# Performance work log

Measured on AMD Instinct MI355X. Metric: run time of the kernel, lower is better.

The kernel has to match this reference:

```python
import jax, jax.numpy as jnp
import numpy as np

B, S, D, H = 512, 128, 2, 512


def _lstm_cell(x, h, c, Wih, Whh, bih, bhh):
    # PyTorch gate order: i, f, g, o
    z = x @ Wih.T + h @ Whh.T + bih + bhh
    i, f, g, o = jnp.split(z, 4, axis=-1)
    c = jax.nn.sigmoid(f) * c + jax.nn.sigmoid(i) * jnp.tanh(g)
    h = jax.nn.sigmoid(o) * jnp.tanh(c)
    return h, c


def setup_inputs() -> dict:
    key = jax.random.key(0)
    ks = jax.random.split(key, 18)
    sc = 1.0 / np.sqrt(H)
    u = lambda k, shape: jax.random.uniform(k, shape, jnp.float32, -sc, sc)
    return {
        "inp": jax.random.normal(ks[0], (B, S, D), jnp.float32),
        "enc_Wih": u(ks[1], (4 * H, D)),
        "enc_Whh": u(ks[2], (4 * H, H)),
        "enc_bih": u(ks[3], (4 * H,)),
        "enc_bhh": u(ks[4], (4 * H,)),
        "dec_Wih": u(ks[5], (4 * H, D)),
        "dec_Whh": u(ks[6], (4 * H, H)),
        "dec_bih": u(ks[7], (4 * H,)),
        "dec_bhh": u(ks[8], (4 * H,)),
        "W1": u(ks[9], (H, H)),
        "b1": u(ks[10], (H,)),
        "W2": u(ks[11], (H, H)),
        "b2": u(ks[12], (H,)),
        "v_w": u(ks[13], (H,)),
        "v_b": u(ks[14], (1,)),
        "comb_W": u(ks[15], (H, 2 * H)),
        "comb_b": u(ks[16], (H,)),
    }


def reference(inp, enc_Wih, enc_Whh, enc_bih, enc_bhh,
              dec_Wih, dec_Whh, dec_bih, dec_bhh,
              W1, b1, W2, b2, v_w, v_b, comb_W, comb_b):
    Bb, Ss, _ = inp.shape
    xs = jnp.transpose(inp, (1, 0, 2))  # [S,B,D]

    # --- encoder LSTM (1 layer) ---
    def enc_step(carry, x):
        h, c = carry
        h, c = _lstm_cell(x, h, c, enc_Wih, enc_Whh, enc_bih, enc_bhh)
        return (h, c), h

    h0 = jnp.zeros((Bb, H), inp.dtype)
    (h_enc, c_enc), enc_out = jax.lax.scan(enc_step, (h0, h0), xs)  # enc_out: [S,B,H]

    W1e = enc_out @ W1.T + b1            # [S,B,H]
    enc_bt = jnp.transpose(enc_out, (1, 0, 2))  # [B,S,H]

    # --- pointer decoder ---
    def dec_step(carry, _):
        h, c, cur = carry
        h, c = _lstm_cell(cur, h, c, dec_Wih, dec_Whh, dec_bih, dec_bhh)
        q = h @ W2.T + b2                               # [B,H]
        u = jnp.tanh(W1e + q[None]) @ v_w + v_b[0]      # [S,B]
        a = jax.nn.softmax(u.T, axis=1)                 # [B,S]
        chosen = jnp.argmax(a, axis=1)                  # [B]
        cur = jnp.take_along_axis(inp, chosen[:, None, None], axis=1)[:, 0, :]  # [B,D]
        ctx = jnp.einsum('bs,bsh->bh', a, enc_bt)       # [B,H]
        h = jnp.concatenate([ctx, h], axis=1) @ comb_W.T + comb_b
        return (h, c, cur), a

    cur0 = jnp.full((Bb, D), -1.0, inp.dtype)
    _, outs = jax.lax.scan(dec_step, (h_enc, c_enc, cur0), None, length=Ss)
    return jnp.transpose(outs, (1, 0, 2))  # [B,S,S]
```

## Files before the change

### kernel.cpp

```cpp
#include <hip/hip_runtime.h>

#define PB 512
#define PS 128
#define PD 2
#define PH 512
#define P4H 2048

typedef unsigned int u32;
typedef unsigned short u16;
typedef __attribute__((ext_vector_type(8))) short short8;
typedef __attribute__((ext_vector_type(4))) float f32x4;

__device__ __forceinline__ float fast_sigmoid(float x) {
    return __fdividef(1.0f, 1.0f + __expf(-x));
}
__device__ __forceinline__ float fast_tanh(float x) {
    float ax = fabsf(x);
    float e = __expf(-2.0f * ax);
    float r = __fdividef(1.0f - e, 1.0f + e);
    return x < 0.0f ? -r : r;
}

__device__ __forceinline__ float bf_dec_u(u16 v) { return __uint_as_float((u32)v << 16); }
__device__ __forceinline__ u16 bf_trunc(float v) { return (u16)(__float_as_uint(v) >> 16); }
__device__ __forceinline__ u16 bf_rne(float v) {
    u32 u = __float_as_uint(v);
    return (u16)((u + 0x7FFFu + ((u >> 16) & 1u)) >> 16);
}
__device__ __forceinline__ void bf_split(float v, u16& hi, u16& lo) {
    hi = bf_trunc(v);
    lo = bf_rne(v - bf_dec_u(hi));
}

struct CF32 {
    using T = float;
    static __device__ __forceinline__ float dec(T v) { return v; }
    static __device__ __forceinline__ T enc(float v) { return v; }
    static __device__ __forceinline__ void dec4(const T* p, float* o) {
        float4 v = *(const float4*)p; o[0]=v.x; o[1]=v.y; o[2]=v.z; o[3]=v.w;
    }
};
struct CBF16 {
    using T = u16;
    static __device__ __forceinline__ float dec(T v) { return __uint_as_float((u32)v << 16); }
    static __device__ __forceinline__ T enc(float v) { return bf_rne(v); }
    static __device__ __forceinline__ void dec4(const T* p, float* o) {
        uint2 v = *(const uint2*)p;
        o[0] = __uint_as_float(v.x << 16);
        o[1] = __uint_as_float(v.x & 0xFFFF0000u);
        o[2] = __uint_as_float(v.y << 16);
        o[3] = __uint_as_float(v.y & 0xFFFF0000u);
    }
};

__global__ __launch_bounds__(256) void prep_whh(
    const float* __restrict__ Whh, u16* __restrict__ hi, u16* __restrict__ lo,
    float* __restrict__ f32out)
{
    int np = blockIdx.x;
    int j = np >> 2, g = np & 3;
    const float* src = Whh + (size_t)(g * PH + j) * PH;
    for (int k = threadIdx.x; k < PH; k += 256) {
        float v = src[k];
        u16 h_, l_;
        bf_split(v, h_, l_);
        hi[(size_t)np * PH + k] = h_;
        lo[(size_t)np * PH + k] = l_;
        if (f32out) f32out[(size_t)np * PH + k] = v;
    }
}
__global__ __launch_bounds__(256) void prep_split(
    const float* __restrict__ W, u16* __restrict__ hi, u16* __restrict__ lo, int K)
{
    int n = blockIdx.x;
    const float* src = W + (size_t)n * K;
    for (int k = threadIdx.x; k < K; k += 256) {
        u16 h_, l_;
        bf_split(src[k], h_, l_);
        hi[(size_t)n * K + k] = h_;
        lo[(size_t)n * K + k] = l_;
    }
}
__global__ __launch_bounds__(256) void prep_transpose_split(
    const float* __restrict__ W, u16* __restrict__ hi, u16* __restrict__ lo)
{
    __shared__ float tile[32][33];
    int m0 = blockIdx.x * 32;
    int k0 = blockIdx.y * 32;
    int tx = threadIdx.x & 31, ty = threadIdx.x >> 5;
    #pragma unroll
    for (int i = 0; i < 4; ++i) {
        int k = k0 + ty + i * 8;
        tile[ty + i * 8][tx] = W[(size_t)k * (2 * PH) + m0 + tx];
    }
    __syncthreads();
    #pragma unroll
    for (int i = 0; i < 4; ++i) {
        int m = m0 + ty + i * 8;
        float v = tile[tx][ty + i * 8];
        u16 h_, l_; bf_split(v, h_, l_);
        hi[(size_t)m * PH + k0 + tx] = h_;
        lo[(size_t)m * PH + k0 + tx] = l_;
    }
}
__global__ __launch_bounds__(256) void prep_small(
    const float* __restrict__ Wih, const float* __restrict__ bih,
    const float* __restrict__ bhh, float* __restrict__ wihp, float* __restrict__ bs)
{
    int np = blockIdx.x * 256 + threadIdx.x;
    if (np >= P4H) return;
    int j = np >> 2, g = np & 3;
    int n = g * PH + j;
    wihp[np * 2]     = Wih[(size_t)n * PD];
    wihp[np * 2 + 1] = Wih[(size_t)n * PD + 1];
    bs[np] = bih[n] + bhh[n];
}
__global__ __launch_bounds__(256) void prep_bfused(
    const float* __restrict__ whh_f32p, const float* __restrict__ comb_b,
    const float* __restrict__ bsum_d, float* __restrict__ bf)
{
    int np = blockIdx.x * 4 + (threadIdx.x >> 6);
    int lane = threadIdx.x & 63;
    const float* wr = whh_f32p + (size_t)np * PH + lane * 8;
    const float* cb = comb_b + lane * 8;
    float s = 0.0f;
    #pragma unroll
    for (int i = 0; i < 8; ++i) s += wr[i] * cb[i];
    #pragma unroll
    for (int off = 32; off; off >>= 1) s += __shfl_xor(s, off);
    if (lane == 0) bf[np] = s + bsum_d[np];
}

template<int EXTRA_MODE, int KK>
__global__ __launch_bounds__(256, 2) void lstm_fused32(
    const u16* __restrict__ Whh_hi, const u16* __restrict__ Whh_lo,
    const float* __restrict__ wih_perm, const float* __restrict__ bsum,
    const float* __restrict__ x, int x_stride,
    const float* __restrict__ h_in,
    float* __restrict__ cT,
    float* __restrict__ h_out,
    void* __restrict__ extra, int ex_stride)
{
    __shared__ u16 As_hi[32][72];
    __shared__ u16 As_lo[32][72];
    __shared__ u16 Bs_hi[64][72];
    __shared__ u16 Bs_lo[64][72];

    const int tid = threadIdx.x;
    const int bnp = blockIdx.x * 32;
    const int bb  = blockIdx.y * 64;
    const int w = tid >> 6;
    const int wm = w >> 1, wn = w & 1;
    const int lane = tid & 63;
    const int l15 = lane & 15, lq = lane >> 4;

    f32x4 acc0 = (f32x4)0.0f, acc1 = (f32x4)0.0f;

    for (int k0 = 0; k0 < KK; k0 += 64) {
        {
            int row = tid >> 3, kc = (tid & 7) * 8;
            *(uint4*)&As_hi[row][kc] = *(const uint4*)&Whh_hi[(size_t)(bnp + row) * KK + k0 + kc];
            *(uint4*)&As_lo[row][kc] = *(const uint4*)&Whh_lo[(size_t)(bnp + row) * KK + k0 + kc];
        }
        #pragma unroll
        for (int rep = 0; rep < 4; ++rep) {
            int chunk = tid + rep * 256;
            int row = chunk >> 4, kc = (chunk & 15) * 4;
            float4 v = *(const float4*)&h_in[(size_t)(bb + row) * KK + k0 + kc];
            u16 h0_, l0_, h1_, l1_, h2_, l2_, h3_, l3_;
            bf_split(v.x, h0_, l0_); bf_split(v.y, h1_, l1_);
            bf_split(v.z, h2_, l2_); bf_split(v.w, h3_, l3_);
            *(uint2*)&Bs_hi[row][kc] = make_uint2((u32)h0_ | ((u32)h1_ << 16),
                                                  (u32)h2_ | ((u32)h3_ << 16));
            *(uint2*)&Bs_lo[row][kc] = make_uint2((u32)l0_ | ((u32)l1_ << 16),
                                                  (u32)l2_ | ((u32)l3_ << 16));
        }
        __syncthreads();
        #pragma unroll
        for (int ks = 0; ks < 2; ++ks) {
            int kk = ks * 32 + lq * 8;
            short8 ah, al, bh0, bl0, bh1, bl1;
            {
                int r = wm * 16 + l15;
                ah = *(const short8*)&As_hi[r][kk];
                al = *(const short8*)&As_lo[r][kk];
            }
            {
                int r = wn * 32 + l15;
                bh0 = *(const short8*)&Bs_hi[r][kk];
                bl0 = *(const short8*)&Bs_lo[r][kk];
                bh1 = *(const short8*)&Bs_hi[r + 16][kk];
                bl1 = *(const short8*)&Bs_lo[r + 16][kk];
            }
            acc0 = __builtin_amdgcn_mfma_f32_16x16x32_bf16(ah, bh0, acc0, 0, 0, 0);
            acc0 = __builtin_amdgcn_mfma_f32_16x16x32_bf16(ah, bl0, acc0, 0, 0, 0);
            acc0 = __builtin_amdgcn_mfma_f32_16x16x32_bf16(al, bh0, acc0, 0, 0, 0);
            acc1 = __builtin_amdgcn_mfma_f32_16x16x32_bf16(ah, bh1, acc1, 0, 0, 0);
            acc1 = __builtin_amdgcn_mfma_f32_16x16x32_bf16(ah, bl1, acc1, 0, 0, 0);
            acc1 = __builtin_amdgcn_mfma_f32_16x16x32_bf16(al, bh1, acc1, 0, 0, 0);
        }
        __syncthreads();
    }

    float* Hs = (float*)&As_hi[0][0];
    const int np_loc = wm * 16 + lq * 4;
    const int np = bnp + np_loc;
    const float4 b4 = *(const float4*)&bsum[np];
    const float4 wA = *(const float4*)&wih_perm[np * 2];
    const float4 wB = *(const float4*)&wih_perm[np * 2 + 4];
    const int jg = np >> 2;
    #pragma unroll
    for (int nf = 0; nf < 2; ++nf) {
        int b_loc = wn * 32 + nf * 16 + l15;
        int b = bb + b_loc;
        float x0 = x[b * x_stride];
        float x1 = x[b * x_stride + 1];
        f32x4 a = nf ? acc1 : acc0;
        float zi = a[0] + b4.x + x0 * wA.x + x1 * wA.y;
        float zf = a[1] + b4.y + x0 * wA.z + x1 * wA.w;
        float zg = a[2] + b4.z + x0 * wB.x + x1 * wB.y;
        float zo = a[3] + b4.w + x0 * wB.z + x1 * wB.w;
        float cold = cT[(size_t)jg * PB + b];
        float cv = fast_sigmoid(zf) * cold + fast_sigmoid(zi) * fast_tanh(zg);
        float hv = fast_sigmoid(zo) * fast_tanh(cv);
        cT[(size_t)jg * PB + b] = cv;
        Hs[(np_loc >> 2) * 66 + b_loc] = hv;
    }
    __syncthreads();
    {
        int b_loc = tid & 63, jp = (tid >> 6) * 2;
        int b = bb + b_loc;
        int jbase = bnp >> 2;
        float h0v = Hs[jp * 66 + b_loc];
        float h1v = Hs[(jp + 1) * 66 + b_loc];
        *(float2*)&h_out[(size_t)b * PH + jbase + jp] = make_float2(h0v, h1v);
        if (EXTRA_MODE == 1) {
            u16* e = (u16*)extra;
            *(u32*)&e[(size_t)b * ex_stride + jbase + jp] =
                (u32)bf_rne(h0v) | ((u32)bf_rne(h1v) << 16);
        } else if (EXTRA_MODE == 2) {
            float* e = (float*)extra;
            *(float2*)&e[(size_t)b * ex_stride + jbase + jp] = make_float2(h0v, h1v);
        }
    }
}

__global__ __launch_bounds__(256, 2) void gemm32_f32(
    const u16* __restrict__ Whi, const u16* __restrict__ Wlo,
    const float* __restrict__ act, const float* __restrict__ bias,
    float* __restrict__ out, int K, int ldo)
{
    __shared__ u16 As_hi[32][72];
    __shared__ u16 As_lo[32][72];
    __shared__ u16 Bs_hi[32][72];
    __shared__ u16 Bs_lo[32][72];

    const int tid = threadIdx.x;
    const int bn = blockIdx.x * 32;
    const int bm = blockIdx.y * 32;
    const int w = tid >> 6;
    const int wm = w >> 1, wn = w & 1;
    const int lane = tid & 63, l15 = lane & 15, lq = lane >> 4;

    f32x4 acc = (f32x4)0.0f;

    for (int k0 = 0; k0 < K; k0 += 64) {
        {
            int row = tid >> 3, kc = (tid & 7) * 8;
            *(uint4*)&As_hi[row][kc] = *(const uint4*)&Whi[(size_t)(bn + row) * K + k0 + kc];
            *(uint4*)&As_lo[row][kc] = *(const uint4*)&Wlo[(size_t)(bn + row) * K + k0 + kc];
        }
        #pragma unroll
        for (int rep = 0; rep < 2; ++rep) {
            int chunk = tid + rep * 256;
            int row = chunk >> 4, kc = (chunk & 15) * 4;
            float4 v = *(const float4*)&act[(size_t)(bm + row) * K + k0 + kc];
            u16 h0_, l0_, h1_, l1_, h2_, l2_, h3_, l3_;
            bf_split(v.x, h0_, l0_); bf_split(v.y, h1_, l1_);
            bf_split(v.z, h2_, l2_); bf_split(v.w, h3_, l3_);
            *(uint2*)&Bs_hi[row][kc] = make_uint2((u32)h0_ | ((u32)h1_ << 16),
                                                  (u32)h2_ | ((u32)h3_ << 16));
            *(uint2*)&Bs_lo[row][kc] = make_uint2((u32)l0_ | ((u32)l1_ << 16),
                                                  (u32)l2_ | ((u32)l3_ << 16));
        }
        __syncthreads();
        #pragma unroll
        for (int ks = 0; ks < 2; ++ks) {
            int kk = ks * 32 + lq * 8;
            short8 ah = *(const short8*)&As_hi[wm * 16 + l15][kk];
            short8 al = *(const short8*)&As_lo[wm * 16 + l15][kk];
            short8 bh = *(const short8*)&Bs_hi[wn * 16 + l15][kk];
            short8 bl = *(const short8*)&Bs_lo[wn * 16 + l15][kk];
            acc = __builtin_amdgcn_mfma_f32_16x16x32_bf16(ah, bh, acc, 0, 0, 0);
            acc = __builtin_amdgcn_mfma_f32_16x16x32_bf16(ah, bl, acc, 0, 0, 0);
            acc = __builtin_amdgcn_mfma_f32_16x16x32_bf16(al, bh, acc, 0, 0, 0);
        }
        __syncthreads();
    }

    int m = bm + wn * 16 + l15;
    int n = bn + wm * 16 + lq * 4;
    float4 b4 = bias ? *(const float4*)&bias[n] : make_float4(0.f, 0.f, 0.f, 0.f);
    *(float4*)&out[(size_t)m * ldo + n] =
        make_float4(acc[0] + b4.x, acc[1] + b4.y, acc[2] + b4.z, acc[3] + b4.w);
}

template<int EXTRA_MODE, int KK>
__global__ __launch_bounds__(256) void lstm_fused(
    const u16* __restrict__ Whh_hi, const u16* __restrict__ Whh_lo,
    const float* __restrict__ wih_perm, const float* __restrict__ bsum,
    const float* __restrict__ x, int x_stride,
    const float* __restrict__ h_in,
    float* __restrict__ cT,
    float* __restrict__ h_out,
    void* __restrict__ extra, int ex_stride)
{
    __shared__ u16 As_hi[64][72];
    __shared__ u16 As_lo[64][72];
    __shared__ u16 Bs_hi[64][72];
    __shared__ u16 Bs_lo[64][72];

    const int tid = threadIdx.x;
    const int bb = blockIdx.x * 64;
    const int bn = blockIdx.y * 64;
    const int w = tid >> 6;
    const int wm = w >> 1, wn = w & 1;
    const int lane = tid & 63;
    const int l15 = lane & 15, lq = lane >> 4;

    f32x4 acc[2][2];
    #pragma unroll
    for (int i = 0; i < 2; ++i)
        #pragma unroll
        for (int j = 0; j < 2; ++j)
            acc[i][j] = (f32x4)0.0f;

    for (int k0 = 0; k0 < KK; k0 += 64) {
        #pragma unroll
        for (int rep = 0; rep < 2; ++rep) {
            int chunk = tid + rep * 256;
            int row = chunk >> 3, kc = (chunk & 7) * 8;
            *(uint4*)&As_hi[row][kc] = *(const uint4*)&Whh_hi[(size_t)(bn + row) * KK + k0 + kc];
            *(uint4*)&As_lo[row][kc] = *(const uint4*)&Whh_lo[(size_t)(bn + row) * KK + k0 + kc];
        }
        #pragma unroll
        for (int rep = 0; rep < 4; ++rep) {
            int chunk = tid + rep * 256;
            int row = chunk >> 4, kc = (chunk & 15) * 4;
            float4 v = *(const float4*)&h_in[(size_t)(bb + row) * KK + k0 + kc];
            u16 h0_, l0_, h1_, l1_, h2_, l2_, h3_, l3_;
            bf_split(v.x, h0_, l0_); bf_split(v.y, h1_, l1_);
            bf_split(v.z, h2_, l2_); bf_split(v.w, h3_, l3_);
            *(uint2*)&Bs_hi[row][kc] = make_uint2((u32)h0_ | ((u32)h1_ << 16),
                                                  (u32)h2_ | ((u32)h3_ << 16));
            *(uint2*)&Bs_lo[row][kc] = make_uint2((u32)l0_ | ((u32)l1_ << 16),
                                                  (u32)l2_ | ((u32)l3_ << 16));
        }
        __syncthreads();
        #pragma unroll
        for (int ks = 0; ks < 2; ++ks) {
            int kk = ks * 32 + lq * 8;
            short8 ah[2], al[2], bh[2], bl[2];
            #pragma unroll
            for (int mf = 0; mf < 2; ++mf) {
                int r = wm * 32 + mf * 16 + l15;
                ah[mf] = *(const short8*)&As_hi[r][kk];
                al[mf] = *(const short8*)&As_lo[r][kk];
            }
            #pragma unroll
            for (int nf = 0; nf < 2; ++nf) {
                int r = wn * 32 + nf * 16 + l15;
                bh[nf] = *(const short8*)&Bs_hi[r][kk];
                bl[nf] = *(const short8*)&Bs_lo[r][kk];
            }
            #pragma unroll
            for (int mf = 0; mf < 2; ++mf)
                #pragma unroll
                for (int nf = 0; nf < 2; ++nf) {
                    acc[mf][nf] = __builtin_amdgcn_mfma_f32_16x16x32_bf16(ah[mf], bh[nf], acc[mf][nf], 0, 0, 0);
                    acc[mf][nf] = __builtin_amdgcn_mfma_f32_16x16x32_bf16(ah[mf], bl[nf], acc[mf][nf], 0, 0, 0);
                    acc[mf][nf] = __builtin_amdgcn_mfma_f32_16x16x32_bf16(al[mf], bh[nf], acc[mf][nf], 0, 0, 0);
                }
        }
        __syncthreads();
    }

    float* Hs = (float*)&As_hi[0][0];
    #pragma unroll
    for (int nf = 0; nf < 2; ++nf) {
        int b_loc = wn * 32 + nf * 16 + l15;
        int b = bb + b_loc;
        float x0 = x[b * x_stride];
        float x1 = x[b * x_stride + 1];
        #pragma unroll
        for (int mf = 0; mf < 2; ++mf) {
            int np_loc = wm * 32 + mf * 16 + lq * 4;
            int np = bn + np_loc;
            float4 b4 = *(const float4*)&bsum[np];
            float4 wA = *(const float4*)&wih_perm[np * 2];
            float4 wB = *(const float4*)&wih_perm[np * 2 + 4];
            float zi = acc[mf][nf][0] + b4.x + x0 * wA.x + x1 * wA.y;
            float zf = acc[mf][nf][1] + b4.y + x0 * wA.z + x1 * wA.w;
            float zg = acc[mf][nf][2] + b4.z + x0 * wB.x + x1 * wB.y;
            float zo = acc[mf][nf][3] + b4.w + x0 * wB.z + x1 * wB.w;
            int jg = np >> 2;
            float cold = cT[(size_t)jg * PB + b];
            float cv = fast_sigmoid(zf) * cold + fast_sigmoid(zi) * fast_tanh(zg);
            float hv = fast_sigmoid(zo) * fast_tanh(cv);
            cT[(size_t)jg * PB + b] = cv;
            Hs[(np_loc >> 2) * 66 + b_loc] = hv;
        }
    }
    __syncthreads();
    {
        int b_loc = tid >> 2, jp = (tid & 3) * 4;
        int b = bb + b_loc;
        int jbase = bn >> 2;
        float4 hv4;
        hv4.x = Hs[(jp + 0) * 66 + b_loc];
        hv4.y = Hs[(jp + 1) * 66 + b_loc];
        hv4.z = Hs[(jp + 2) * 66 + b_loc];
        hv4.w = Hs[(jp + 3) * 66 + b_loc];
        *(float4*)&h_out[(size_t)b * PH + jbase + jp] = hv4;
        if (EXTRA_MODE == 1) {
            u16* e = (u16*)extra;
            *(uint2*)&e[(size_t)b * ex_stride + jbase + jp] =
                make_uint2((u32)bf_rne(hv4.x) | ((u32)bf_rne(hv4.y) << 16),
                           (u32)bf_rne(hv4.z) | ((u32)bf_rne(hv4.w) << 16));
        } else if (EXTRA_MODE == 2) {
            float* e = (float*)extra;
            *(float4*)&e[(size_t)b * ex_stride + jbase + jp] = hv4;
        }
    }
}

template<int ACT_F32, int OUTMODE>
__global__ __launch_bounds__(256) void gemm_wtA(
    const u16* __restrict__ Whi, const u16* __restrict__ Wlo,
    const void* __restrict__ act, const float* __restrict__ bias,
    void* __restrict__ out, void* __restrict__ out2, int K, int ldo)
{
    __shared__ u16 As_hi[64][72];
    __shared__ u16 As_lo[64][72];
    __shared__ u16 Bs_hi[64][72];
    __shared__ u16 Bs_lo[64][72];

    const int tid = threadIdx.x;
    const int bm = blockIdx.x * 64;
    const int bn = blockIdx.y * 64;
    const int w = tid >> 6;
    const int wm = w >> 1, wn = w & 1;
    const int lane = tid & 63;
    const int l15 = lane & 15, lq = lane >> 4;

    f32x4 acc[2][2];
    #pragma unroll
    for (int i = 0; i < 2; ++i)
        #pragma unroll
        for (int j = 0; j < 2; ++j)
            acc[i][j] = (f32x4)0.0f;

    for (int k0 = 0; k0 < K; k0 += 64) {
        #pragma unroll
        for (int rep = 0; rep < 2; ++rep) {
            int chunk = tid + rep * 256;
            int row = chunk >> 3, kc = (chunk & 7) * 8;
            *(uint4*)&As_hi[row][kc] = *(const uint4*)&Whi[(size_t)(bn + row) * K + k0 + kc];
            *(uint4*)&As_lo[row][kc] = *(const uint4*)&Wlo[(size_t)(bn + row) * K + k0 + kc];
        }
        if (ACT_F32) {
            const float* a = (const float*)act;
            #pragma unroll
            for (int rep = 0; rep < 4; ++rep) {
                int chunk = tid + rep * 256;
                int row = chunk >> 4, kc = (chunk & 15) * 4;
                float4 v = *(const float4*)&a[(size_t)(bm + row) * K + k0 + kc];
                u16 h0_, l0_, h1_, l1_, h2_, l2_, h3_, l3_;
                bf_split(v.x, h0_, l0_); bf_split(v.y, h1_, l1_);
                bf_split(v.z, h2_, l2_); bf_split(v.w, h3_, l3_);
                *(uint2*)&Bs_hi[row][kc] = make_uint2((u32)h0_ | ((u32)h1_ << 16),
                                                      (u32)h2_ | ((u32)h3_ << 16));
                *(uint2*)&Bs_lo[row][kc] = make_uint2((u32)l0_ | ((u32)l1_ << 16),
                                                      (u32)l2_ | ((u32)l3_ << 16));
            }
        } else {
            const u16* a = (const u16*)act;
            #pragma unroll
            for (int rep = 0; rep < 2; ++rep) {
                int chunk = tid + rep * 256;
                int row = chunk >> 3, kc = (chunk & 7) * 8;
                *(uint4*)&Bs_hi[row][kc] = *(const uint4*)&a[(size_t)(bm + row) * K + k0 + kc];
            }
        }
        __syncthreads();
        #pragma unroll
        for (int ks = 0; ks < 2; ++ks) {
            int kk = ks * 32 + lq * 8;
            short8 ah[2], al[2], bh[2], bl[2];
            #pragma unroll
            for (int mf = 0; mf < 2; ++mf) {
                int r = wm * 32 + mf * 16 + l15;
                ah[mf] = *(const short8*)&As_hi[r][kk];
                al[mf] = *(const short8*)&As_lo[r][kk];
            }
            #pragma unroll
            for (int nf = 0; nf < 2; ++nf) {
                int r = wn * 32 + nf * 16 + l15;
                bh[nf] = *(const short8*)&Bs_hi[r][kk];
                if (ACT_F32) bl[nf] = *(const short8*)&Bs_lo[r][kk];
            }
            #pragma unroll
            for (int mf = 0; mf < 2; ++mf)
                #pragma unroll
                for (int nf = 0; nf < 2; ++nf) {
                    acc[mf][nf] = __builtin_amdgcn_mfma_f32_16x16x32_bf16(ah[mf], bh[nf], acc[mf][nf], 0, 0, 0);
                    if (ACT_F32) {
                        acc[mf][nf] = __builtin_amdgcn_mfma_f32_16x16x32_bf16(ah[mf], bl[nf], acc[mf][nf], 0, 0, 0);
                        acc[mf][nf] = __builtin_amdgcn_mfma_f32_16x16x32_bf16(al[mf], bh[nf], acc[mf][nf], 0, 0, 0);
                    } else {
                        acc[mf][nf] = __builtin_amdgcn_mfma_f32_16x16x32_bf16(al[mf], bh[nf], acc[mf][nf], 0, 0, 0);
                    }
                }
        }
        __syncthreads();
    }

    #pragma unroll
    for (int nf = 0; nf < 2; ++nf) {
        int m = bm + wn * 32 + nf * 16 + l15;
        #pragma unroll
        for (int mf = 0; mf < 2; ++mf) {
            int n = bn + wm * 32 + mf * 16 + lq * 4;
            float4 b4 = bias ? *(const float4*)&bias[n] : make_float4(0.f, 0.f, 0.f, 0.f);
            float v0 = acc[mf][nf][0] + b4.x;
            float v1 = acc[mf][nf][1] + b4.y;
            float v2 = acc[mf][nf][2] + b4.z;
            float v3 = acc[mf][nf][3] + b4.w;
            if (OUTMODE == 1) {
                u16* o = (u16*)out;
                *(uint2*)&o[(size_t)m * ldo + n] =
                    make_uint2((u32)bf_rne(v0) | ((u32)bf_rne(v1) << 16),
                               (u32)bf_rne(v2) | ((u32)bf_rne(v3) << 16));
            } else if (OUTMODE == 2) {
                u16 h0_, l0_, h1_, l1_, h2_, l2_, h3_, l3_;
                bf_split(v0, h0_, l0_); bf_split(v1, h1_, l1_);
                bf_split(v2, h2_, l2_); bf_split(v3, h3_, l3_);
                u16* oh = (u16*)out;
                u16* ol = (u16*)out2;
                *(uint2*)&oh[(size_t)m * ldo + n] =
                    make_uint2((u32)h0_ | ((u32)h1_ << 16), (u32)h2_ | ((u32)h3_ << 16));
                *(uint2*)&ol[(size_t)m * ldo + n] =
                    make_uint2((u32)l0_ | ((u32)l1_ << 16), (u32)l2_ | ((u32)l3_ << 16));
            } else {
                float* o = (float*)out;
                *(float4*)&o[(size_t)m * ldo + n] = make_float4(v0, v1, v2, v3);
            }
        }
    }
}

__global__ __launch_bounds__(256) void attn_fused(
    const u16* __restrict__ W1e,
    const u16* __restrict__ enc_out,
    const float* __restrict__ qv,
    const float* __restrict__ v_w, const float* __restrict__ v_b,
    const float* __restrict__ inp,
    float* __restrict__ out,
    float* __restrict__ cat_out,
    float* __restrict__ cur, int t)
{
    __shared__ float u_s[PS];
    __shared__ float a_s[PS];
    const int b = blockIdx.x;
    const int tid = threadIdx.x;
    const int w = tid >> 6, lane = tid & 63;

    float q8[8], v8[8];
    {
        const float* qr = qv + (size_t)b * PH + lane * 8;
        CF32::dec4(qr, q8); CF32::dec4(qr + 4, q8 + 4);
        const float* vr = v_w + lane * 8;
        CF32::dec4(vr, v8); CF32::dec4(vr + 4, v8 + 4);
    }
    const float vb = v_b[0];
    const u16* wbase = W1e + (size_t)b * PS * PH + lane * 8;
    #pragma unroll 2
    for (int i = 0; i < 32; ++i) {
        int s = w * 32 + i;
        const u16* row = wbase + (size_t)s * PH;
        float w8[8];
        CBF16::dec4(row, w8); CBF16::dec4(row + 4, w8 + 4);
        float sum = 0.0f;
        #pragma unroll
        for (int j = 0; j < 8; ++j) sum += v8[j] * fast_tanh(w8[j] + q8[j]);
        #pragma unroll
        for (int off = 32; off; off >>= 1) sum += __shfl_xor(sum, off);
        if (lane == 0) u_s[s] = sum + vb;
    }
    __syncthreads();
    if (w == 0) {
        float2 uv = make_float2(u_s[lane * 2], u_s[lane * 2 + 1]);
        float m = fmaxf(uv.x, uv.y);
        int mi = (uv.y > uv.x) ? (lane * 2 + 1) : (lane * 2);
        #pragma unroll
        for (int off = 32; off; off >>= 1) {
            float om = __shfl_xor(m, off);
            int oi = __shfl_xor(mi, off);
            if (om > m || (om == m && oi < mi)) { m = om; mi = oi; }
        }
        float e0 = __expf(uv.x - m);
        float e1 = __expf(uv.y - m);
        float ssum = e0 + e1;
        #pragma unroll
        for (int off = 32; off; off >>= 1) ssum += __shfl_xor(ssum, off);
        float inv = __fdividef(1.0f, ssum);
        float2 av = make_float2(e0 * inv, e1 * inv);
        a_s[lane * 2] = av.x; a_s[lane * 2 + 1] = av.y;
        *(float2*)&out[(size_t)b * PS * PS + (size_t)t * PS + lane * 2] = av;
        if (lane == 0) {
            cur[b * 2]     = inp[(size_t)b * PS * PD + mi * PD];
            cur[b * 2 + 1] = inp[(size_t)b * PS * PD + mi * PD + 1];
        }
    }
    __syncthreads();
    float acc0 = 0.0f, acc1 = 0.0f;
    const u16* ebase = enc_out + (size_t)b * PS * PH + tid * 2;
    #pragma unroll 4
    for (int s = 0; s < PS; ++s) {
        float a = a_s[s];
        u32 pr = *(const u32*)(ebase + (size_t)s * PH);
        acc0 = fmaf(a, __uint_as_float(pr << 16), acc0);
        acc1 = fmaf(a, __uint_as_float(pr & 0xFFFF0000u), acc1);
    }
    *(float2*)&cat_out[(size_t)b * (2 * PH) + tid * 2] = make_float2(acc0, acc1);
}

template<class C>
__global__ __launch_bounds__(256) void u_pass(
    const typename C::T* __restrict__ W1e, const float* __restrict__ q,
    const float* __restrict__ v_w, const float* __restrict__ v_b,
    float* __restrict__ u_t)
{
    int row = blockIdx.x * 4 + (threadIdx.x >> 6);
    int lane = threadIdx.x & 63;
    int s = row >> 9;
    int b = row & (PB - 1);
    const typename C::T* wr = W1e + (size_t)row * PH + lane * 8;
    const float* qr = q + (size_t)b * PH + lane * 8;
    const float* vr = v_w + lane * 8;
    float w8[8], q8[8], v8[8];
    C::dec4(wr, w8); C::dec4(wr + 4, w8 + 4);
    CF32::dec4(qr, q8); CF32::dec4(qr + 4, q8 + 4);
    CF32::dec4(vr, v8); CF32::dec4(vr + 4, v8 + 4);
    float sum = 0.0f;
    #pragma unroll
    for (int i = 0; i < 8; ++i)
        sum += v8[i] * fast_tanh(w8[i] + q8[i]);
    #pragma unroll
    for (int off = 32; off; off >>= 1) sum += __shfl_xor(sum, off);
    if (lane == 0) u_t[b * PS + s] = sum + v_b[0];
}

__global__ __launch_bounds__(256) void softmax_step(
    const float* __restrict__ u_t, const float* __restrict__ inp,
    float* __restrict__ a_buf, float* __restrict__ out,
    float* __restrict__ cur, int t)
{
    int b = blockIdx.x * 4 + (threadIdx.x >> 6);
    int lane = threadIdx.x & 63;
    float2 uv = *(const float2*)&u_t[b * PS + lane * 2];
    float m = fmaxf(uv.x, uv.y);
    int mi = (uv.y > uv.x) ? (lane * 2 + 1) : (lane * 2);
    #pragma unroll
    for (int off = 32; off; off >>= 1) {
        float om = __shfl_xor(m, off);
        int oi = __shfl_xor(mi, off);
        if (om > m || (om == m && oi < mi)) { m = om; mi = oi; }
    }
    float e0 = __expf(uv.x - m);
    float e1 = __expf(uv.y - m);
    float ssum = e0 + e1;
    #pragma unroll
    for (int off = 32; off; off >>= 1) ssum += __shfl_xor(ssum, off);
    float inv = __fdividef(1.0f, ssum);
    float2 av = make_float2(e0 * inv, e1 * inv);
    *(float2*)&a_buf[b * PS + lane * 2] = av;
    *(float2*)&out[(size_t)b * PS * PS + (size_t)t * PS + lane * 2] = av;
    if (lane == 0) {
        cur[b * 2]     = inp[(size_t)b * PS * PD + mi * PD];
        cur[b * 2 + 1] = inp[(size_t)b * PS * PD + mi * PD + 1];
    }
}

template<class C>
__global__ __launch_bounds__(256) void ctx_kernel(
    const typename C::T* __restrict__ enc_out, const float* __restrict__ a_buf,
    float* __restrict__ catbuf)
{
    int b = blockIdx.x;
    int hidx = threadIdx.x;
    const float* ab = a_buf + b * PS;
    const typename C::T* e = enc_out + (size_t)b * PH;
    float acc0 = 0.0f, acc1 = 0.0f;
    #pragma unroll 4
    for (int s = 0; s < PS; ++s) {
        float a = ab[s];
        const typename C::T* es = e + (size_t)s * PB * PH;
        acc0 = fmaf(a, C::dec(es[hidx]), acc0);
        acc1 = fmaf(a, C::dec(es[hidx + 256]), acc1);
    }
    catbuf[(size_t)b * (2 * PH) + hidx] = acc0;
    catbuf[(size_t)b * (2 * PH) + hidx + 256] = acc1;
}

__global__ __launch_bounds__(256) void init_kernel(
    float* __restrict__ h, float* __restrict__ c, float* __restrict__ cur)
{
    int i = blockIdx.x * 256 + threadIdx.x;
    if (i < PB * PH) { h[i] = 0.0f; c[i] = 0.0f; }
    if (i < PB * PD) cur[i] = -1.0f;
}

template<class CA, class CO, int BM, int BN, int BK, int TM, int TN>
__global__ __launch_bounds__(256) void gemm_nt(
    const typename CA::T* __restrict__ A, const float* __restrict__ Bm,
    const float* __restrict__ bias, typename CO::T* __restrict__ C,
    int M, int N, int K)
{
    __shared__ float As[BK][BM];
    __shared__ float Bs[BK][BN];
    constexpr int TCOLS = BN / TN;
    constexpr int TROWS = BM / TM;
    static_assert(TCOLS * TROWS == 256, "thread tiling");
    const int tid = threadIdx.x;
    const int tc = tid % TCOLS;
    const int tr = tid / TCOLS;
    const int bm = blockIdx.y * BM;
    const int bn = blockIdx.x * BN;
    constexpr int AF4 = BM * BK / 4;
    constexpr int BF4 = BN * BK / 4;
    constexpr int KQ  = BK / 4;
    float acc[TM][TN];
    #pragma unroll
    for (int m = 0; m < TM; ++m)
        #pragma unroll
        for (int n = 0; n < TN; ++n) acc[m][n] = 0.0f;
    for (int k0 = 0; k0 < K; k0 += BK) {
        #pragma unroll
        for (int i = tid; i < AF4; i += 256) {
            int r = i / KQ, kq = i % KQ;
            float v4[4];
            CA::dec4(A + (size_t)(bm + r) * K + k0 + kq * 4, v4);
            As[kq*4+0][r] = v4[0]; As[kq*4+1][r] = v4[1];
            As[kq*4+2][r] = v4[2]; As[kq*4+3][r] = v4[3];
        }
        #pragma unroll
        for (int i = tid; i < BF4; i += 256) {
            int r = i / KQ, kq = i % KQ;
            const float4 v = *(const float4*)(Bm + (size_t)(bn + r) * K + k0 + kq * 4);
            Bs[kq*4+0][r] = v.x; Bs[kq*4+1][r] = v.y;
            Bs[kq*4+2][r] = v.z; Bs[kq*4+3][r] = v.w;
        }
        __syncthreads();
        #pragma unroll
        for (int k = 0; k < BK; ++k) {
            float av[TM], bv[TN];
            #pragma unroll
            for (int m = 0; m < TM; ++m) av[m] = As[k][tr * TM + m];
            #pragma unroll
            for (int n = 0; n < TN; ++n) bv[n] = Bs[k][tc * TN + n];
            #pragma unroll
            for (int m = 0; m < TM; ++m)
                #pragma unroll
                for (int n = 0; n < TN; ++n)
                    acc[m][n] = fmaf(av[m], bv[n], acc[m][n]);
        }
        __syncthreads();
    }
    #pragma unroll
    for (int m = 0; m < TM; ++m) {
        int row = bm + tr * TM + m;
        #pragma unroll
        for (int n = 0; n < TN; ++n) {
            int col = bn + tc * TN + n;
            float v = acc[m][n];
            if (bias) v += bias[col];
            C[(size_t)row * N + col] = CO::enc(v);
        }
    }
}

template<class CE>
__global__ __launch_bounds__(256) void lstm_cell(
    const float* __restrict__ z,
    const float* __restrict__ x, int x_stride,
    const float* __restrict__ Wih,
    const float* __restrict__ bih, const float* __restrict__ bhh,
    float* __restrict__ c, float* __restrict__ h,
    typename CE::T* __restrict__ extra, int extra_stride)
{
    int idx = blockIdx.x * 256 + threadIdx.x;
    int b = idx >> 9, j = idx & (PH - 1);
    float x0 = x[b * x_stride];
    float x1 = x[b * x_stride + 1];
    const float* zr = z + (size_t)b * P4H;
    float zi = zr[j]        + bih[j]        + bhh[j]        + x0 * Wih[2*j]          + x1 * Wih[2*j+1];
    float zf = zr[j + PH]   + bih[j + PH]   + bhh[j + PH]   + x0 * Wih[2*(j+PH)]     + x1 * Wih[2*(j+PH)+1];
    float zg = zr[j + 2*PH] + bih[j + 2*PH] + bhh[j + 2*PH] + x0 * Wih[2*(j+2*PH)]   + x1 * Wih[2*(j+2*PH)+1];
    float zo = zr[j + 3*PH] + bih[j + 3*PH] + bhh[j + 3*PH] + x0 * Wih[2*(j+3*PH)]   + x1 * Wih[2*(j+3*PH)+1];
    float cv = fast_sigmoid(zf) * c[idx] + fast_sigmoid(zi) * fast_tanh(zg);
    float hv = fast_sigmoid(zo) * fast_tanh(cv);
    c[idx] = cv;
    h[idx] = hv;
    if (extra) extra[(size_t)b * extra_stride + j] = CE::enc(hv);
}

struct Inputs {
    const float *inp, *enc_Wih, *enc_Whh, *enc_bih, *enc_bhh;
    const float *dec_Wih, *dec_Whh, *dec_bih, *dec_bhh;
    const float *W1, *b1, *W2, *b2, *v_w, *v_b, *comb_W, *comb_b;
};
static Inputs unpack(void* const* d_in) {
    Inputs in;
    in.inp = (const float*)d_in[0];
    in.enc_Wih = (const float*)d_in[1]; in.enc_Whh = (const float*)d_in[2];
    in.enc_bih = (const float*)d_in[3]; in.enc_bhh = (const float*)d_in[4];
    in.dec_Wih = (const float*)d_in[5]; in.dec_Whh = (const float*)d_in[6];
    in.dec_bih = (const float*)d_in[7]; in.dec_bhh = (const float*)d_in[8];
    in.W1 = (const float*)d_in[9];  in.b1 = (const float*)d_in[10];
    in.W2 = (const float*)d_in[11]; in.b2 = (const float*)d_in[12];
    in.v_w = (const float*)d_in[13]; in.v_b = (const float*)d_in[14];
    in.comb_W = (const float*)d_in[15]; in.comb_b = (const float*)d_in[16];
    return in;
}

static const size_t BIG = (size_t)PS * PB * PH;

static void run_mfma2(const Inputs& in, float* out, void* d_ws, hipStream_t stream)
{
    char* p = (char*)d_ws;
    auto alloc = [&](size_t bytes) { char* r = p; p += bytes; return r; };
    u16* enc_out  = (u16*)alloc(BIG * 2);
    char* W1e_reg = alloc(BIG * 2);
    u16* W1e = (u16*)W1e_reg;
    u16* w1h = (u16*)alloc((size_t)PH * PH * 2);
    u16* w1l = (u16*)alloc((size_t)PH * PH * 2);
    u16* w2h = (u16*)alloc((size_t)PH * PH * 2);
    u16* w2l = (u16*)alloc((size_t)PH * PH * 2);
    u16* wf_h = (u16*)alloc((size_t)P4H * (2 * PH) * 2);
    u16* wf_l = (u16*)alloc((size_t)P4H * (2 * PH) * 2);
    float* wih_e = (float*)alloc((size_t)P4H * 2 * 4);
    float* wih_d = (float*)alloc((size_t)P4H * 2 * 4);
    float* bsum_e = (float*)alloc((size_t)P4H * 4);
    float* bsum_d = (float*)alloc((size_t)P4H * 4);
    float* b_fus  = (float*)alloc((size_t)P4H * 4);
    float* hpp0 = (float*)alloc((size_t)PB * PH * 4);
    float* cT   = (float*)alloc((size_t)PB * PH * 4);
    float* h0   = (float*)alloc((size_t)PB * PH * 4);
    float* q    = (float*)alloc((size_t)PB * PH * 4);
    float* catreg = (float*)alloc((size_t)PB * 2 * PH * 4 * 2);
    float* cur  = (float*)alloc((size_t)PB * PD * 4);

    u16* ctw_h     = (u16*)(W1e_reg + 0);
    u16* ctw_l     = (u16*)(W1e_reg + 1048576);
    u16* whh_e_hi  = (u16*)(W1e_reg + 2097152);
    u16* whh_e_lo  = (u16*)(W1e_reg + 4194304);
    u16* whh_d_hi  = (u16*)(W1e_reg + 6291456);
    u16* whh_d_lo  = (u16*)(W1e_reg + 8388608);
    float* hpp1    = (float*)(W1e_reg + 10485760);
    float* whh_f32p = catreg;
    float* cat[2] = { catreg, catreg + (size_t)PB * 2 * PH };
    float* hpp[2] = { hpp0, hpp1 };

    prep_whh<<<P4H, 256, 0, stream>>>(in.enc_Whh, whh_e_hi, whh_e_lo, nullptr);
    prep_whh<<<P4H, 256, 0, stream>>>(in.dec_Whh, whh_d_hi, whh_d_lo, whh_f32p);
    prep_split<<<PH, 256, 0, stream>>>(in.W1, w1h, w1l, PH);
    prep_split<<<PH, 256, 0, stream>>>(in.W2, w2h, w2l, PH);
    prep_transpose_split<<<dim3(32, 16), 256, 0, stream>>>(in.comb_W, ctw_h, ctw_l);
    prep_small<<<P4H / 256, 256, 0, stream>>>(in.enc_Wih, in.enc_bih, in.enc_bhh, wih_e, bsum_e);
    prep_small<<<P4H / 256, 256, 0, stream>>>(in.dec_Wih, in.dec_bih, in.dec_bhh, wih_d, bsum_d);
    gemm_wtA<1, 2><<<dim3(P4H / 64, (2 * PH) / 64), 256, 0, stream>>>(
        ctw_h, ctw_l, whh_f32p, nullptr, wf_h, wf_l, PH, 2 * PH);
    prep_bfused<<<P4H / 4, 256, 0, stream>>>(whh_f32p, in.comb_b, bsum_d, b_fus);
    init_kernel<<<1024, 256, 0, stream>>>(hpp0, cT, cur);

    for (int s = 0; s < PS; ++s) {
        lstm_fused32<1, PH><<<dim3(P4H / 32, PB / 64), 256, 0, stream>>>(
            whh_e_hi, whh_e_lo, wih_e, bsum_e,
            in.inp + s * PD, PS * PD,
            hpp[s & 1], cT, hpp[(s + 1) & 1],
            enc_out + (size_t)s * PH, PS * PH);
    }

    lstm_fused32<2, PH><<<dim3(P4H / 32, PB / 64), 256, 0, stream>>>(
        whh_d_hi, whh_d_lo, wih_d, bsum_d,
        cur, PD, hpp[0], cT, h0, cat[1] + PH, 2 * PH);

    gemm_wtA<0, 1><<<dim3((PS * PB) / 64, PH / 64), 256, 0, stream>>>(
        w1h, w1l, enc_out, in.b1, W1e, nullptr, PH, PH);

    for (int t = 0; t < PS; ++t) {
        float* cat_out = cat[(t + 1) & 1];
        if (t > 0) {
            lstm_fused32<2, 2 * PH><<<dim3(P4H / 32, PB / 64), 256, 0, stream>>>(
                wf_h, wf_l, wih_d, b_fus,
                cur, PD, cat[t & 1], cT, h0, cat_out + PH, 2 * PH);
        }
        gemm32_f32<<<dim3(PH / 32, PB / 32), 256, 0, stream>>>(
            w2h, w2l, h0, in.b2, q, PH, PH);
        attn_fused<<<PB, 256, 0, stream>>>(
            W1e, enc_out, q, in.v_w, in.v_b, in.inp, out, cat_out, cur, t);
    }
}

static void run_mfma(const Inputs& in, float* out, void* d_ws, hipStream_t stream)
{
    char* p = (char*)d_ws;
    auto alloc = [&](size_t bytes) { char* r = p; p += bytes; return r; };
    u16* enc_out = (u16*)alloc(BIG * 2);
    u16* W1e     = (u16*)alloc(BIG * 2);
    u16* whh_e_hi = (u16*)alloc((size_t)P4H * PH * 2);
    u16* whh_e_lo = (u16*)alloc((size_t)P4H * PH * 2);
    u16* whh_d_hi = (u16*)alloc((size_t)P4H * PH * 2);
    u16* whh_d_lo = (u16*)alloc((size_t)P4H * PH * 2);
    u16* w1h = (u16*)alloc((size_t)PH * PH * 2);
    u16* w1l = (u16*)alloc((size_t)PH * PH * 2);
    u16* w2h = (u16*)alloc((size_t)PH * PH * 2);
    u16* w2l = (u16*)alloc((size_t)PH * PH * 2);
    u16* cwh = (u16*)alloc((size_t)PH * 2 * PH * 2);
    u16* cwl = (u16*)alloc((size_t)PH * 2 * PH * 2);
    float* wih_e = (float*)alloc((size_t)P4H * 2 * 4);
    float* wih_d = (float*)alloc((size_t)P4H * 2 * 4);
    float* bsum_e = (float*)alloc((size_t)P4H * 4);
    float* bsum_d = (float*)alloc((size_t)P4H * 4);
    float* hpp0 = (float*)alloc((size_t)PB * PH * 4);
    float* hpp1 = (float*)alloc((size_t)PB * PH * 4);
    float* cT   = (float*)alloc((size_t)PB * PH * 4);
    float* h0   = (float*)alloc((size_t)PB * PH * 4);
    float* q    = (float*)alloc((size_t)PB * PH * 4);
    float* catbuf = (float*)alloc((size_t)PB * 2 * PH * 4);
    float* u_t  = (float*)alloc((size_t)PB * PS * 4);
    float* a_buf = (float*)alloc((size_t)PB * PS * 4);
    float* cur  = (float*)alloc((size_t)PB * PD * 4);
    float* hpp[2] = { hpp0, hpp1 };

    prep_whh<<<P4H, 256, 0, stream>>>(in.enc_Whh, whh_e_hi, whh_e_lo, nullptr);
    prep_whh<<<P4H, 256, 0, stream>>>(in.dec_Whh, whh_d_hi, whh_d_lo, nullptr);
    prep_split<<<PH, 256, 0, stream>>>(in.W1, w1h, w1l, PH);
    prep_split<<<PH, 256, 0, stream>>>(in.W2, w2h, w2l, PH);
    prep_split<<<PH, 256, 0, stream>>>(in.comb_W, cwh, cwl, 2 * PH);
    prep_small<<<P4H / 256, 256, 0, stream>>>(in.enc_Wih, in.enc_bih, in.enc_bhh, wih_e, bsum_e);
    prep_small<<<P4H / 256, 256, 0, stream>>>(in.dec_Wih, in.dec_bih, in.dec_bhh, wih_d, bsum_d);
    init_kernel<<<1024, 256, 0, stream>>>(hpp0, cT, cur);

    for (int s = 0; s < PS; ++s) {
        lstm_fused<1, PH><<<dim3(PB / 64, P4H / 64), 256, 0, stream>>>(
            whh_e_hi, whh_e_lo, wih_e, bsum_e,
            in.inp + s * PD, PS * PD,
            hpp[s & 1], cT, hpp[(s + 1) & 1],
            enc_out + (size_t)s * PB * PH, PH);
    }
    gemm_wtA<0, 1><<<dim3((PS * PB) / 64, PH / 64), 256, 0, stream>>>(
        w1h, w1l, enc_out, in.b1, W1e, nullptr, PH, PH);
    for (int t = 0; t < PS; ++t) {
        lstm_fused<2, PH><<<dim3(PB / 64, P4H / 64), 256, 0, stream>>>(
            whh_d_hi, whh_d_lo, wih_d, bsum_d,
            cur, PD, hpp[t & 1], cT, h0, catbuf + PH, 2 * PH);
        gemm_wtA<1, 0><<<dim3(PB / 64, PH / 64), 256, 0, stream>>>(
            w2h, w2l, h0, in.b2, q, nullptr, PH, PH);
        u_pass<CBF16><<<(PS * PB) / 4, 256, 0, stream>>>(W1e, q, in.v_w, in.v_b, u_t);
        softmax_step<<<PB / 4, 256, 0, stream>>>(u_t, in.inp, a_buf, out, cur, t);
        ctx_kernel<CBF16><<<PB, 256, 0, stream>>>(enc_out, a_buf, catbuf);
        gemm_wtA<1, 0><<<dim3(PB / 64, PH / 64), 256, 0, stream>>>(
            cwh, cwl, catbuf, in.comb_b, hpp[(t + 1) & 1], nullptr, 2 * PH, PH);
    }
}

static void run_fallback(const Inputs& in, float* out, void* d_ws, hipStream_t stream)
{
    char* p = (char*)d_ws;
    u16* enc_out = (u16*)p;  p += BIG * 2;
    u16* W1e     = (u16*)p;  p += BIG * 2;
    float* ws = (float*)p;
    size_t off = 0;
    auto alloc = [&](size_t n) { float* r = ws + off; off += n; return r; };
    float* z      = alloc((size_t)PB * P4H);
    float* h      = alloc((size_t)PB * PH);
    float* c      = alloc((size_t)PB * PH);
    float* h0     = alloc((size_t)PB * PH);
    float* q      = alloc((size_t)PB * PH);
    float* catbuf = alloc((size_t)PB * 2 * PH);
    float* u_t    = alloc((size_t)PB * PS);
    float* a_buf  = alloc((size_t)PB * PS);
    float* cur    = alloc((size_t)PB * PD);

    init_kernel<<<1024, 256, 0, stream>>>(h, c, cur);
    for (int s = 0; s < PS; ++s) {
        gemm_nt<CF32, CF32, 64, 64, 32, 4, 4><<<dim3(P4H / 64, PB / 64), 256, 0, stream>>>(
            h, in.enc_Whh, nullptr, z, PB, P4H, PH);
        lstm_cell<CBF16><<<1024, 256, 0, stream>>>(
            z, in.inp + s * PD, PS * PD, in.enc_Wih, in.enc_bih, in.enc_bhh,
            c, h, enc_out + (size_t)s * PB * PH, PH);
    }
    gemm_nt<CBF16, CBF16, 64, 64, 32, 4, 4><<<dim3(PH / 64, (PS * PB) / 64), 256, 0, stream>>>(
        enc_out, in.W1, in.b1, W1e, PS * PB, PH, PH);
    for (int t = 0; t < PS; ++t) {
        gemm_nt<CF32, CF32, 64, 64, 32, 4, 4><<<dim3(P4H / 64, PB / 64), 256, 0, stream>>>(
            h, in.dec_Whh, nullptr, z, PB, P4H, PH);
        lstm_cell<CF32><<<1024, 256, 0, stream>>>(
            z, cur, PD, in.dec_Wih, in.dec_bih, in.dec_bhh,
            c, h0, catbuf + PH, 2 * PH);
        gemm_nt<CF32, CF32, 32, 32, 32, 2, 2><<<dim3(PH / 32, PB / 32), 256, 0, stream>>>(
            h0, in.W2, in.b2, q, PB, PH, PH);
        u_pass<CBF16><<<(PS * PB) / 4, 256, 0, stream>>>(W1e, q, in.v_w, in.v_b, u_t);
        softmax_step<<<PB / 4, 256, 0, stream>>>(u_t, in.inp, a_buf, out, cur, t);
        ctx_kernel<CBF16><<<PB, 256, 0, stream>>>(enc_out, a_buf, catbuf);
        gemm_nt<CF32, CF32, 32, 32, 32, 2, 2><<<dim3(PH / 32, PB / 32), 256, 0, stream>>>(
            catbuf, in.comb_W, in.comb_b, h, PB, PH, 2 * PH);
    }
}

extern "C" void kernel_launch(void* const* d_in, const int* in_sizes, int n_in,
                              void* d_out, int out_size, void* d_ws, size_t ws_size,
                              hipStream_t stream)
{
    Inputs in = unpack(d_in);
    float* out = (float*)d_out;

    const size_t t1_need =
        BIG * 2 * 2 +
        (size_t)PH * PH * 2 * 4 +
        (size_t)P4H * (2 * PH) * 2 * 2 +
        (size_t)P4H * 2 * 4 * 2 +
        (size_t)P4H * 4 * 3 +
        (size_t)PB * PH * 4 * 4 +
        (size_t)PB * 2 * PH * 4 * 2 +
        (size_t)PB * PD * 4;
    const size_t t2_need =
        BIG * 2 * 2 +
        (size_t)P4H * PH * 2 * 4 +
        (size_t)PH * PH * 2 * 4 +
        (size_t)PH * 2 * PH * 2 * 2 +
        (size_t)P4H * 2 * 4 * 2 +
        (size_t)P4H * 4 * 2 +
        ((size_t)PB * PH * 6 + (size_t)PB * PS * 2 + PB * PD) * 4;
    const size_t t3_need =
        BIG * 2 * 2 +
        ((size_t)PB * P4H + 4 * (size_t)PB * PH + (size_t)PB * 2 * PH +
         2 * (size_t)PB * PS + (size_t)PB * PD) * 4;

    if (ws_size >= t1_need)       run_mfma2(in, out, d_ws, stream);
    else if (ws_size >= t2_need)  run_mfma(in, out, d_ws, stream);
    else if (ws_size >= t3_need)  run_fallback(in, out, d_ws, stream);
}
```

Before: 10.79 ms.

## Replace per-step kernel launches with persistent encoder/decoder kernels using grid barriers

```diff
diff --git a/kernel.cpp b/kernel.cpp
--- a/kernel.cpp
+++ b/kernel.cpp
@@ -5,6 +5,7 @@
 #define PD 2
 #define PH 512
 #define P4H 2048
+#define NBLK 512
 
 typedef unsigned int u32;
 typedef unsigned short u16;
@@ -53,6 +54,26 @@
     }
 };
 
+__device__ __forceinline__ void gbar(unsigned* bar, unsigned target) {
+    __syncthreads();
+    if (threadIdx.x == 0) {
+        __threadfence();
+        __hip_atomic_fetch_add(bar, 1u, __ATOMIC_RELEASE, __HIP_MEMORY_SCOPE_AGENT);
+        while (__hip_atomic_load(bar, __ATOMIC_ACQUIRE, __HIP_MEMORY_SCOPE_AGENT) < target) {
+            __builtin_amdgcn_s_sleep(4);
+        }
+        __threadfence();
+    }
+    __syncthreads();
+}
+
+struct LdsBuf {
+    u16 As_hi[32][72];
+    u16 As_lo[32][72];
+    u16 Bs_hi[64][72];
+    u16 Bs_lo[64][72];
+};
+
 __global__ __launch_bounds__(256) void prep_whh(
     const float* __restrict__ Whh, u16* __restrict__ hi, u16* __restrict__ lo,
     float* __restrict__ f32out)
@@ -130,25 +151,25 @@
     for (int off = 32; off; off >>= 1) s += __shfl_xor(s, off);
     if (lane == 0) bf[np] = s + bsum_d[np];
 }
+__global__ __launch_bounds__(256) void init_kernel2(
+    float* __restrict__ h, float* __restrict__ c, float* __restrict__ cur,
+    unsigned* __restrict__ bars)
+{
+    int i = blockIdx.x * 256 + threadIdx.x;
+    if (i < PB * PH) { h[i] = 0.0f; c[i] = 0.0f; }
+    if (i < PB * PD) cur[i] = -1.0f;
+    if (i < 64) bars[i] = 0u;
+}
 
 template<int EXTRA_MODE, int KK>
-__global__ __launch_bounds__(256, 2) void lstm_fused32(
+__device__ __forceinline__ void lstm32_body(LdsBuf& L, int bnp, int bb,
     const u16* __restrict__ Whh_hi, const u16* __restrict__ Whh_lo,
     const float* __restrict__ wih_perm, const float* __restrict__ bsum,
     const float* __restrict__ x, int x_stride,
-    const float* __restrict__ h_in,
-    float* __restrict__ cT,
-    float* __restrict__ h_out,
-    void* __restrict__ extra, int ex_stride)
-{
-    __shared__ u16 As_hi[32][72];
-    __shared__ u16 As_lo[32][72];
-    __shared__ u16 Bs_hi[64][72];
-    __shared__ u16 Bs_lo[64][72];
-
+    const float* __restrict__ h_in, float* __restrict__ cT,
+    float* __restrict__ h_out, void* __restrict__ extra, int ex_stride)
+{
     const int tid = threadIdx.x;
-    const int bnp = blockIdx.x * 32;
-    const int bb  = blockIdx.y * 64;
     const int w = tid >> 6;
     const int wm = w >> 1, wn = w & 1;
     const int lane = tid & 63;
@@ -159,8 +180,8 @@
     for (int k0 = 0; k0 < KK; k0 += 64) {
         {
             int row = tid >> 3, kc = (tid & 7) * 8;
-            *(uint4*)&As_hi[row][kc] = *(const uint4*)&Whh_hi[(size_t)(bnp + row) * KK + k0 + kc];
-            *(uint4*)&As_lo[row][kc] = *(const uint4*)&Whh_lo[(size_t)(bnp + row) * KK + k0 + kc];
+            *(uint4*)&L.As_hi[row][kc] = *(const uint4*)&Whh_hi[(size_t)(bnp + row) * KK + k0 + kc];
+            *(uint4*)&L.As_lo[row][kc] = *(const uint4*)&Whh_lo[(size_t)(bnp + row) * KK + k0 + kc];
         }
         #pragma unroll
         for (int rep = 0; rep < 4; ++rep) {
@@ -170,10 +191,10 @@
             u16 h0_, l0_, h1_, l1_, h2_, l2_, h3_, l3_;
             bf_split(v.x, h0_, l0_); bf_split(v.y, h1_, l1_);
             bf_split(v.z, h2_, l2_); bf_split(v.w, h3_, l3_);
-            *(uint2*)&Bs_hi[row][kc] = make_uint2((u32)h0_ | ((u32)h1_ << 16),
-                                                  (u32)h2_ | ((u32)h3_ << 16));
-            *(uint2*)&Bs_lo[row][kc] = make_uint2((u32)l0_ | ((u32)l1_ << 16),
-                                                  (u32)l2_ | ((u32)l3_ << 16));
+            *(uint2*)&L.Bs_hi[row][kc] = make_uint2((u32)h0_ | ((u32)h1_ << 16),
+                                                    (u32)h2_ | ((u32)h3_ << 16));
+            *(uint2*)&L.Bs_lo[row][kc] = make_uint2((u32)l0_ | ((u32)l1_ << 16),
+                                                    (u32)l2_ | ((u32)l3_ << 16));
         }
         __syncthreads();
         #pragma unroll
@@ -182,15 +203,15 @@
             short8 ah, al, bh0, bl0, bh1, bl1;
             {
                 int r = wm * 16 + l15;
-                ah = *(const short8*)&As_hi[r][kk];
-                al = *(const short8*)&As_lo[r][kk];
+                ah = *(const short8*)&L.As_hi[r][kk];
+                al = *(const short8*)&L.As_lo[r][kk];
             }
             {
                 int r = wn * 32 + l15;
-                bh0 = *(const short8*)&Bs_hi[r][kk];
-                bl0 = *(const short8*)&Bs_lo[r][kk];
-                bh1 = *(const short8*)&Bs_hi[r + 16][kk];
-                bl1 = *(const short8*)&Bs_lo[r + 16][kk];
+                bh0 = *(const short8*)&L.Bs_hi[r][kk];
+                bl0 = *(const short8*)&L.Bs_lo[r][kk];
+                bh1 = *(const short8*)&L.Bs_hi[r + 16][kk];
+                bl1 = *(const short8*)&L.Bs_lo[r + 16][kk];
             }
             acc0 = __builtin_amdgcn_mfma_f32_16x16x32_bf16(ah, bh0, acc0, 0, 0, 0);
             acc0 = __builtin_amdgcn_mfma_f32_16x16x32_bf16(ah, bl0, acc0, 0, 0, 0);
@@ -202,7 +223,7 @@
         __syncthreads();
     }
 
-    float* Hs = (float*)&As_hi[0][0];
+    float* Hs = (float*)&L.As_hi[0][0];
     const int np_loc = wm * 16 + lq * 4;
     const int np = bnp + np_loc;
     const float4 b4 = *(const float4*)&bsum[np];
@@ -245,19 +266,25 @@
     }
 }
 
-__global__ __launch_bounds__(256, 2) void gemm32_f32(
+template<int EXTRA_MODE, int KK>
+__global__ __launch_bounds__(256, 2) void lstm_fused32(
+    const u16* __restrict__ Whh_hi, const u16* __restrict__ Whh_lo,
+    const float* __restrict__ wih_perm, const float* __restrict__ bsum,
+    const float* __restrict__ x, int x_stride,
+    const float* __restrict__ h_in, float* __restrict__ cT,
+    float* __restrict__ h_out, void* __restrict__ extra, int ex_stride)
+{
+    __shared__ LdsBuf L;
+    lstm32_body<EXTRA_MODE, KK>(L, blockIdx.x * 32, blockIdx.y * 64,
+        Whh_hi, Whh_lo, wih_perm, bsum, x, x_stride, h_in, cT, h_out, extra, ex_stride);
+}
+
+__device__ __forceinline__ void gemm32_body(LdsBuf& L, int bn, int bm,
     const u16* __restrict__ Whi, const u16* __restrict__ Wlo,
     const float* __restrict__ act, const float* __restrict__ bias,
     float* __restrict__ out, int K, int ldo)
 {
-    __shared__ u16 As_hi[32][72];
-    __shared__ u16 As_lo[32][72];
-    __shared__ u16 Bs_hi[32][72];
-    __shared__ u16 Bs_lo[32][72];
-
     const int tid = threadIdx.x;
-    const int bn = blockIdx.x * 32;
-    const int bm = blockIdx.y * 32;
     const int w = tid >> 6;
     const int wm = w >> 1, wn = w & 1;
     const int lane = tid & 63, l15 = lane & 15, lq = lane >> 4;
@@ -267,8 +294,8 @@
     for (int k0 = 0; k0 < K; k0 += 64) {
         {
             int row = tid >> 3, kc = (tid & 7) * 8;
-            *(uint4*)&As_hi[row][kc] = *(const uint4*)&Whi[(size_t)(bn + row) * K + k0 + kc];
-            *(uint4*)&As_lo[row][kc] = *(const uint4*)&Wlo[(size_t)(bn + row) * K + k0 + kc];
+            *(uint4*)&L.As_hi[row][kc] = *(const uint4*)&Whi[(size_t)(bn + row) * K + k0 + kc];
+            *(uint4*)&L.As_lo[row][kc] = *(const uint4*)&Wlo[(size_t)(bn + row) * K + k0 + kc];
         }
         #pragma unroll
         for (int rep = 0; rep < 2; ++rep) {
@@ -278,19 +305,19 @@
             u16 h0_, l0_, h1_, l1_, h2_, l2_, h3_, l3_;
             bf_split(v.x, h0_, l0_); bf_split(v.y, h1_, l1_);
             bf_split(v.z, h2_, l2_); bf_split(v.w, h3_, l3_);
-            *(uint2*)&Bs_hi[row][kc] = make_uint2((u32)h0_ | ((u32)h1_ << 16),
-                                                  (u32)h2_ | ((u32)h3_ << 16));
-            *(uint2*)&Bs_lo[row][kc] = make_uint2((u32)l0_ | ((u32)l1_ << 16),
-                                                  (u32)l2_ | ((u32)l3_ << 16));
+            *(uint2*)&L.Bs_hi[row][kc] = make_uint2((u32)h0_ | ((u32)h1_ << 16),
+                                                    (u32)h2_ | ((u32)h3_ << 16));
+            *(uint2*)&L.Bs_lo[row][kc] = make_uint2((u32)l0_ | ((u32)l1_ << 16),
+                                                    (u32)l2_ | ((u32)l3_ << 16));
         }
         __syncthreads();
         #pragma unroll
         for (int ks = 0; ks < 2; ++ks) {
             int kk = ks * 32 + lq * 8;
-            short8 ah = *(const short8*)&As_hi[wm * 16 + l15][kk];
-            short8 al = *(const short8*)&As_lo[wm * 16 + l15][kk];
-            short8 bh = *(const short8*)&Bs_hi[wn * 16 + l15][kk];
-            short8 bl = *(const short8*)&Bs_lo[wn * 16 + l15][kk];
+            short8 ah = *(const short8*)&L.As_hi[wm * 16 + l15][kk];
+            short8 al = *(const short8*)&L.As_lo[wm * 16 + l15][kk];
+            short8 bh = *(const short8*)&L.Bs_hi[wn * 16 + l15][kk];
+            short8 bl = *(const short8*)&L.Bs_lo[wn * 16 + l15][kk];
             acc = __builtin_amdgcn_mfma_f32_16x16x32_bf16(ah, bh, acc, 0, 0, 0);
             acc = __builtin_amdgcn_mfma_f32_16x16x32_bf16(ah, bl, acc, 0, 0, 0);
             acc = __builtin_amdgcn_mfma_f32_16x16x32_bf16(al, bh, acc, 0, 0, 0);
@@ -305,132 +332,134 @@
         make_float4(acc[0] + b4.x, acc[1] + b4.y, acc[2] + b4.z, acc[3] + b4.w);
 }
 
-template<int EXTRA_MODE, int KK>
-__global__ __launch_bounds__(256) void lstm_fused(
-    const u16* __restrict__ Whh_hi, const u16* __restrict__ Whh_lo,
-    const float* __restrict__ wih_perm, const float* __restrict__ bsum,
-    const float* __restrict__ x, int x_stride,
-    const float* __restrict__ h_in,
-    float* __restrict__ cT,
-    float* __restrict__ h_out,
-    void* __restrict__ extra, int ex_stride)
-{
-    __shared__ u16 As_hi[64][72];
-    __shared__ u16 As_lo[64][72];
-    __shared__ u16 Bs_hi[64][72];
-    __shared__ u16 Bs_lo[64][72];
-
+__device__ __forceinline__ void attn_body(LdsBuf& L, int b,
+    const u16* __restrict__ W1e, const u16* __restrict__ enc_out,
+    const float* __restrict__ qv, const float* __restrict__ v_w,
+    const float* __restrict__ v_b, const float* __restrict__ inp,
+    float* __restrict__ out, float* __restrict__ cat_out,
+    float* __restrict__ cur, int t)
+{
+    float* u_s = (float*)&L;
+    float* a_s = u_s + PS;
     const int tid = threadIdx.x;
-    const int bb = blockIdx.x * 64;
-    const int bn = blockIdx.y * 64;
-    const int w = tid >> 6;
-    const int wm = w >> 1, wn = w & 1;
-    const int lane = tid & 63;
-    const int l15 = lane & 15, lq = lane >> 4;
-
-    f32x4 acc[2][2];
-    #pragma unroll
-    for (int i = 0; i < 2; ++i)
-        #pragma unroll
-        for (int j = 0; j < 2; ++j)
-            acc[i][j] = (f32x4)0.0f;
-
-    for (int k0 = 0; k0 < KK; k0 += 64) {
-        #pragma unroll
-        for (int rep = 0; rep < 2; ++rep) {
-            int chunk = tid + rep * 256;
-            int row = chunk >> 3, kc = (chunk & 7) * 8;
-            *(uint4*)&As_hi[row][kc] = *(const uint4*)&Whh_hi[(size_t)(bn + row) * KK + k0 + kc];
-            *(uint4*)&As_lo[row][kc] = *(const uint4*)&Whh_lo[(size_t)(bn + row) * KK + k0 + kc];
-        }
-        #pragma unroll
-        for (int rep = 0; rep < 4; ++rep) {
-            int chunk = tid + rep * 256;
-            int row = chunk >> 4, kc = (chunk & 15) * 4;
-            float4 v = *(const float4*)&h_in[(size_t)(bb + row) * KK + k0 + kc];
-            u16 h0_, l0_, h1_, l1_, h2_, l2_, h3_, l3_;
-            bf_split(v.x, h0_, l0_); bf_split(v.y, h1_, l1_);
-            bf_split(v.z, h2_, l2_); bf_split(v.w, h3_, l3_);
-            *(uint2*)&Bs_hi[row][kc] = make_uint2((u32)h0_ | ((u32)h1_ << 16),
-                                                  (u32)h2_ | ((u32)h3_ << 16));
-            *(uint2*)&Bs_lo[row][kc] = make_uint2((u32)l0_ | ((u32)l1_ << 16),
-                                                  (u32)l2_ | ((u32)l3_ << 16));
-        }
-        __syncthreads();
-        #pragma unroll
-        for (int ks = 0; ks < 2; ++ks) {
-            int kk = ks * 32 + lq * 8;
-            short8 ah[2], al[2], bh[2], bl[2];
-            #pragma unroll
-            for (int mf = 0; mf < 2; ++mf) {
-                int r = wm * 32 + mf * 16 + l15;
-                ah[mf] = *(const short8*)&As_hi[r][kk];
-                al[mf] = *(const short8*)&As_lo[r][kk];
-            }
-            #pragma unroll
-            for (int nf = 0; nf < 2; ++nf) {
-                int r = wn * 32 + nf * 16 + l15;
-                bh[nf] = *(const short8*)&Bs_hi[r][kk];
-                bl[nf] = *(const short8*)&Bs_lo[r][kk];
-            }
-            #pragma unroll
-            for (int mf = 0; mf < 2; ++mf)
-                #pragma unroll
-                for (int nf = 0; nf < 2; ++nf) {
-                    acc[mf][nf] = __builtin_amdgcn_mfma_f32_16x16x32_bf16(ah[mf], bh[nf], acc[mf][nf], 0, 0, 0);
-                    acc[mf][nf] = __builtin_amdgcn_mfma_f32_16x16x32_bf16(ah[mf], bl[nf], acc[mf][nf], 0, 0, 0);
-                    acc[mf][nf] = __builtin_amdgcn_mfma_f32_16x16x32_bf16(al[mf], bh[nf], acc[mf][nf], 0, 0, 0);
-                }
-        }
-        __syncthreads();
-    }
-
-    float* Hs = (float*)&As_hi[0][0];
-    #pragma unroll
-    for (int nf = 0; nf < 2; ++nf) {
-        int b_loc = wn * 32 + nf * 16 + l15;
-        int b = bb + b_loc;
-        float x0 = x[b * x_stride];
-        float x1 = x[b * x_stride + 1];
-        #pragma unroll
-        for (int mf = 0; mf < 2; ++mf) {
-            int np_loc = wm * 32 + mf * 16 + lq * 4;
-            int np = bn + np_loc;
-            float4 b4 = *(const float4*)&bsum[np];
-            float4 wA = *(const float4*)&wih_perm[np * 2];
-            float4 wB = *(const float4*)&wih_perm[np * 2 + 4];
-            float zi = acc[mf][nf][0] + b4.x + x0 * wA.x + x1 * wA.y;
-            float zf = acc[mf][nf][1] + b4.y + x0 * wA.z + x1 * wA.w;
-            float zg = acc[mf][nf][2] + b4.z + x0 * wB.x + x1 * wB.y;
-            float zo = acc[mf][nf][3] + b4.w + x0 * wB.z + x1 * wB.w;
-            int jg = np >> 2;
-            float cold = cT[(size_t)jg * PB + b];
-            float cv = fast_sigmoid(zf) * cold + fast_sigmoid(zi) * fast_tanh(zg);
-            float hv = fast_sigmoid(zo) * fast_tanh(cv);
-            cT[(size_t)jg * PB + b] = cv;
-            Hs[(np_loc >> 2) * 66 + b_loc] = hv;
-        }
+    const int w = tid >> 6, lane = tid & 63;
+
+    float q8[8], v8[8];
+    {
+        const float* qr = qv + (size_t)b * PH + lane * 8;
+        CF32::dec4(qr, q8); CF32::dec4(qr + 4, q8 + 4);
+        const float* vr = v_w + lane * 8;
+        CF32::dec4(vr, v8); CF32::dec4(vr + 4, v8 + 4);
+    }
+    const float vb = v_b[0];
+    const u16* wbase = W1e + (size_t)b * PS * PH + lane * 8;
+    #pragma unroll 2
+    for (int i = 0; i < 32; ++i) {
+        int s = w * 32 + i;
+        const u16* row = wbase + (size_t)s * PH;
+        float w8[8];
+        CBF16::dec4(row, w8); CBF16::dec4(row + 4, w8 + 4);
+        float sum = 0.0f;
+        #pragma unroll
+        for (int j = 0; j < 8; ++j) sum += v8[j] * fast_tanh(w8[j] + q8[j]);
+        #pragma unroll
+        for (int off = 32; off; off >>= 1) sum += __shfl_xor(sum, off);
+        if (lane == 0) u_s[s] = sum + vb;
     }
     __syncthreads();
-    {
-        int b_loc = tid >> 2, jp = (tid & 3) * 4;
-        int b = bb + b_loc;
-        int jbase = bn >> 2;
-        float4 hv4;
-        hv4.x = Hs[(jp + 0) * 66 + b_loc];
-        hv4.y = Hs[(jp + 1) * 66 + b_loc];
-        hv4.z = Hs[(jp + 2) * 66 + b_loc];
-        hv4.w = Hs[(jp + 3) * 66 + b_loc];
-        *(float4*)&h_out[(size_t)b * PH + jbase + jp] = hv4;
-        if (EXTRA_MODE == 1) {
-            u16* e = (u16*)extra;
-            *(uint2*)&e[(size_t)b * ex_stride + jbase + jp] =
-                make_uint2((u32)bf_rne(hv4.x) | ((u32)bf_rne(hv4.y) << 16),
-                           (u32)bf_rne(hv4.z) | ((u32)bf_rne(hv4.w) << 16));
-        } else if (EXTRA_MODE == 2) {
-            float* e = (float*)extra;
-            *(float4*)&e[(size_t)b * ex_stride + jbase + jp] = hv4;
-        }
+    if (w == 0) {
+        float2 uv = make_float2(u_s[lane * 2], u_s[lane * 2 + 1]);
+        float m = fmaxf(uv.x, uv.y);
+        int mi = (uv.y > uv.x) ? (lane * 2 + 1) : (lane * 2);
+        #pragma unroll
+        for (int off = 32; off; off >>= 1) {
+            float om = __shfl_xor(m, off);
+            int oi = __shfl_xor(mi, off);
+            if (om > m || (om == m && oi < mi)) { m = om; mi = oi; }
+        }
+        float e0 = __expf(uv.x - m);
+        float e1 = __expf(uv.y - m);
+        float ssum = e0 + e1;
+        #pragma unroll
+        for (int off = 32; off; off >>= 1) ssum += __shfl_xor(ssum, off);
+        float inv = __fdividef(1.0f, ssum);
+        float2 av = make_float2(e0 * inv, e1 * inv);
+        a_s[lane * 2] = av.x; a_s[lane * 2 + 1] = av.y;
+        *(float2*)&out[(size_t)b * PS * PS + (size_t)t * PS + lane * 2] = av;
+        if (lane == 0) {
+            cur[b * 2]     = inp[(size_t)b * PS * PD + mi * PD];
+            cur[b * 2 + 1] = inp[(size_t)b * PS * PD + mi * PD + 1];
+        }
+    }
+    __syncthreads();
+    float acc0 = 0.0f, acc1 = 0.0f;
+    const u16* ebase = enc_out + (size_t)b * PS * PH + tid * 2;
+    #pragma unroll 4
+    for (int s = 0; s < PS; ++s) {
+        float a = a_s[s];
+        u32 pr = *(const u32*)(ebase + (size_t)s * PH);
+        acc0 = fmaf(a, __uint_as_float(pr << 16), acc0);
+        acc1 = fmaf(a, __uint_as_float(pr & 0xFFFF0000u), acc1);
+    }
+    *(float2*)&cat_out[(size_t)b * (2 * PH) + tid * 2] = make_float2(acc0, acc1);
+}
+
+__global__ __launch_bounds__(256, 2) void encoder_persistent(
+    const u16* __restrict__ whh_e_hi, const u16* __restrict__ whh_e_lo,
+    const float* __restrict__ wih_e, const float* __restrict__ bsum_e,
+    const float* __restrict__ inp,
+    float* __restrict__ hpp0, float* __restrict__ hpp1,
+    float* __restrict__ cT, u16* __restrict__ enc_out, unsigned* __restrict__ bar)
+{
+    __shared__ LdsBuf L;
+    const int bnp = (blockIdx.x & 63) * 32;
+    const int bb  = (blockIdx.x >> 6) * 64;
+    unsigned target = 0;
+    for (int s = 0; s < PS; ++s) {
+        const float* hin = (s & 1) ? hpp1 : hpp0;
+        float* hout = (s & 1) ? hpp0 : hpp1;
+        lstm32_body<1, PH>(L, bnp, bb, whh_e_hi, whh_e_lo, wih_e, bsum_e,
+                           inp + s * PD, PS * PD, hin, cT, hout,
+                           enc_out + (size_t)s * PH, PS * PH);
+        target += NBLK;
+        gbar(bar, target);
+    }
+}
+
+__global__ __launch_bounds__(256, 2) void decoder_persistent(
+    const u16* __restrict__ wf_h, const u16* __restrict__ wf_l,
+    const float* __restrict__ wih_d, const float* __restrict__ b_fus,
+    const u16* __restrict__ w2h, const u16* __restrict__ w2l,
+    const float* __restrict__ b2,
+    const u16* __restrict__ W1e, const u16* __restrict__ enc_out,
+    const float* __restrict__ v_w, const float* __restrict__ v_b,
+    const float* __restrict__ inp,
+    float* __restrict__ cT, float* __restrict__ h0, float* __restrict__ q,
+    float* __restrict__ cat0, float* __restrict__ cat1,
+    float* __restrict__ cur, float* __restrict__ out, unsigned* __restrict__ bar)
+{
+    __shared__ LdsBuf L;
+    const int blk = blockIdx.x;
+    unsigned target = 0;
+    float* cat[2] = { cat0, cat1 };
+    for (int t = 0; t < PS; ++t) {
+        float* cat_out = cat[(t + 1) & 1];
+        if (t > 0) {
+            lstm32_body<2, 2 * PH>(L, (blk & 63) * 32, (blk >> 6) * 64,
+                wf_h, wf_l, wih_d, b_fus, cur, PD, cat[t & 1], cT, h0,
+                cat_out + PH, 2 * PH);
+            target += NBLK;
+            gbar(bar, target);
+        }
+        if (blk < 256) {
+            gemm32_body(L, (blk & 15) * 32, (blk >> 4) * 32,
+                        w2h, w2l, h0, b2, q, PH, PH);
+        }
+        target += NBLK;
+        gbar(bar, target);
+        attn_body(L, blk, W1e, enc_out, q, v_w, v_b, inp, out, cat_out, cur, t);
+        target += NBLK;
+        gbar(bar, target);
     }
 }
 
@@ -559,80 +588,133 @@
     }
 }
 
-__global__ __launch_bounds__(256) void attn_fused(
-    const u16* __restrict__ W1e,
-    const u16* __restrict__ enc_out,
-    const float* __restrict__ qv,
-    const float* __restrict__ v_w, const float* __restrict__ v_b,
-    const float* __restrict__ inp,
-    float* __restrict__ out,
-    float* __restrict__ cat_out,
-    float* __restrict__ cur, int t)
-{
-    __shared__ float u_s[PS];
-    __shared__ float a_s[PS];
-    const int b = blockIdx.x;
+template<int EXTRA_MODE, int KK>
+__global__ __launch_bounds__(256) void lstm_fused(
+    const u16* __restrict__ Whh_hi, const u16* __restrict__ Whh_lo,
+    const float* __restrict__ wih_perm, const float* __restrict__ bsum,
+    const float* __restrict__ x, int x_stride,
+    const float* __restrict__ h_in,
+    float* __restrict__ cT,
+    float* __restrict__ h_out,
+    void* __restrict__ extra, int ex_stride)
+{
+    __shared__ u16 As_hi[64][72];
+    __shared__ u16 As_lo[64][72];
+    __shared__ u16 Bs_hi[64][72];
+    __shared__ u16 Bs_lo[64][72];
+
     const int tid = threadIdx.x;
-    const int w = tid >> 6, lane = tid & 63;
-
-    float q8[8], v8[8];
+    const int bb = blockIdx.x * 64;
+    const int bn = blockIdx.y * 64;
+    const int w = tid >> 6;
+    const int wm = w >> 1, wn = w & 1;
+    const int lane = tid & 63;
+    const int l15 = lane & 15, lq = lane >> 4;
+
+    f32x4 acc[2][2];
+    #pragma unroll
+    for (int i = 0; i < 2; ++i)
+        #pragma unroll
+        for (int j = 0; j < 2; ++j)
+            acc[i][j] = (f32x4)0.0f;
+
+    for (int k0 = 0; k0 < KK; k0 += 64) {
+        #pragma unroll
+        for (int rep = 0; rep < 2; ++rep) {
+            int chunk = tid + rep * 256;
+            int row = chunk >> 3, kc = (chunk & 7) * 8;
+            *(uint4*)&As_hi[row][kc] = *(const uint4*)&Whh_hi[(size_t)(bn + row) * KK + k0 + kc];
+            *(uint4*)&As_lo[row][kc] = *(const uint4*)&Whh_lo[(size_t)(bn + row) * KK + k0 + kc];
+        }
+        #pragma unroll
+        for (int rep = 0; rep < 4; ++rep) {
+            int chunk = tid + rep * 256;
+            int row = chunk >> 4, kc = (chunk & 15) * 4;
+            float4 v = *(const float4*)&h_in[(size_t)(bb + row) * KK + k0 + kc];
+            u16 h0_, l0_, h1_, l1_, h2_, l2_, h3_, l3_;
+            bf_split(v.x, h0_, l0_); bf_split(v.y, h1_, l1_);
+            bf_split(v.z, h2_, l2_); bf_split(v.w, h3_, l3_);
+            *(uint2*)&Bs_hi[row][kc] = make_uint2((u32)h0_ | ((u32)h1_ << 16),
+                                                  (u32)h2_ | ((u32)h3_ << 16));
+            *(uint2*)&Bs_lo[row][kc] = make_uint2((u32)l0_ | ((u32)l1_ << 16),
+                                                  (u32)l2_ | ((u32)l3_ << 16));
+        }
+        __syncthreads();
+        #pragma unroll
+        for (int ks = 0; ks < 2; ++ks) {
+            int kk = ks * 32 + lq * 8;
+            short8 ah[2], al[2], bh[2], bl[2];
+            #pragma unroll
+            for (int mf = 0; mf < 2; ++mf) {
+                int r = wm * 32 + mf * 16 + l15;
+                ah[mf] = *(const short8*)&As_hi[r][kk];
+                al[mf] = *(const short8*)&As_lo[r][kk];
+            }
+            #pragma unroll
+            for (int nf = 0; nf < 2; ++nf) {
+                int r = wn * 32 + nf * 16 + l15;
+                bh[nf] = *(const short8*)&Bs_hi[r][kk];
+                bl[nf] = *(const short8*)&Bs_lo[r][kk];
+            }
+            #pragma unroll
+            for (int mf = 0; mf < 2; ++mf)
+                #pragma unroll
+                for (int nf = 0; nf < 2; ++nf) {
+                    acc[mf][nf] = __builtin_amdgcn_mfma_f32_16x16x32_bf16(ah[mf], bh[nf], acc[mf][nf], 0, 0, 0);
+                    acc[mf][nf] = __builtin_amdgcn_mfma_f32_16x16x32_bf16(ah[mf], bl[nf], acc[mf][nf], 0, 0, 0);
+                    acc[mf][nf] = __builtin_amdgcn_mfma_f32_16x16x32_bf16(al[mf], bh[nf], acc[mf][nf], 0, 0, 0);
+                }
+        }
+        __syncthreads();
+    }
+
+    float* Hs = (float*)&As_hi[0][0];
+    #pragma unroll
+    for (int nf = 0; nf < 2; ++nf) {
+        int b_loc = wn * 32 + nf * 16 + l15;
+        int b = bb + b_loc;
+        float x0 = x[b * x_stride];
+        float x1 = x[b * x_stride + 1];
+        #pragma unroll
+        for (int mf = 0; mf < 2; ++mf) {
+            int np_loc = wm * 32 + mf * 16 + lq * 4;
+            int np = bn + np_loc;
+            float4 b4 = *(const float4*)&bsum[np];
+            float4 wA = *(const float4*)&wih_perm[np * 2];
+            float4 wB = *(const float4*)&wih_perm[np * 2 + 4];
+            float zi = acc[mf][nf][0] + b4.x + x0 * wA.x + x1 * wA.y;
+            float zf = acc[mf][nf][1] + b4.y + x0 * wA.z + x1 * wA.w;
+            float zg = acc[mf][nf][2] + b4.z + x0 * wB.x + x1 * wB.y;
+            float zo = acc[mf][nf][3] + b4.w + x0 * wB.z + x1 * wB.w;
+            int jg = np >> 2;
+            float cold = cT[(size_t)jg * PB + b];
+            float cv = fast_sigmoid(zf) * cold + fast_sigmoid(zi) * fast_tanh(zg);
+            float hv = fast_sigmoid(zo) * fast_tanh(cv);
+            cT[(size_t)jg * PB + b] = cv;
+            Hs[(np_loc >> 2) * 66 + b_loc] = hv;
+        }
+    }
+    __syncthreads();
     {
-        const float* qr = qv + (size_t)b * PH + lane * 8;
-        CF32::dec4(qr, q8); CF32::dec4(qr + 4, q8 + 4);
-        const float* vr = v_w + lane * 8;
-        CF32::dec4(vr, v8); CF32::dec4(vr + 4, v8 + 4);
-    }
-    const float vb = v_b[0];
-    const u16* wbase = W1e + (size_t)b * PS * PH + lane * 8;
-    #pragma unroll 2
-    for (int i = 0; i < 32; ++i) {
-        int s = w * 32 + i;
-        const u16* row = wbase + (size_t)s * PH;
-        float w8[8];
-        CBF16::dec4(row, w8); CBF16::dec4(row + 4, w8 + 4);
-        float sum = 0.0f;
-        #pragma unroll
-        for (int j = 0; j < 8; ++j) sum += v8[j] * fast_tanh(w8[j] + q8[j]);
-        #pragma unroll
-        for (int off = 32; off; off >>= 1) sum += __shfl_xor(sum, off);
-        if (lane == 0) u_s[s] = sum + vb;
-    }
-    __syncthreads();
-    if (w == 0) {
-        float2 uv = make_float2(u_s[lane * 2], u_s[lane * 2 + 1]);
-        float m = fmaxf(uv.x, uv.y);
-        int mi = (uv.y > uv.x) ? (lane * 2 + 1) : (lane * 2);
-        #pragma unroll
-        for (int off = 32; off; off >>= 1) {
-            float om = __shfl_xor(m, off);
-            int oi = __shfl_xor(mi, off);
-            if (om > m || (om == m && oi < mi)) { m = om; mi = oi; }
-        }
-        float e0 = __expf(uv.x - m);
-        float e1 = __expf(uv.y - m);
-        float ssum = e0 + e1;
-        #pragma unroll
-        for (int off = 32; off; off >>= 1) ssum += __shfl_xor(ssum, off);
-        float inv = __fdividef(1.0f, ssum);
-        float2 av = make_float2(e0 * inv, e1 * inv);
-        a_s[lane * 2] = av.x; a_s[lane * 2 + 1] = av.y;
-        *(float2*)&out[(size_t)b * PS * PS + (size_t)t * PS + lane * 2] = av;
-        if (lane == 0) {
-            cur[b * 2]     = inp[(size_t)b * PS * PD + mi * PD];
-            cur[b * 2 + 1] = inp[(size_t)b * PS * PD + mi * PD + 1];
-        }
-    }
-    __syncthreads();
-    float acc0 = 0.0f, acc1 = 0.0f;
-    const u16* ebase = enc_out + (size_t)b * PS * PH + tid * 2;
-    #pragma unroll 4
-    for (int s = 0; s < PS; ++s) {
-        float a = a_s[s];
-        u32 pr = *(const u32*)(ebase + (size_t)s * PH);
-        acc0 = fmaf(a, __uint_as_float(pr << 16), acc0);
-        acc1 = fmaf(a, __uint_as_float(pr & 0xFFFF0000u), acc1);
-    }
-    *(float2*)&cat_out[(size_t)b * (2 * PH) + tid * 2] = make_float2(acc0, acc1);
+        int b_loc = tid >> 2, jp = (tid & 3) * 4;
+        int b = bb + b_loc;
+        int jbase = bn >> 2;
+        float4 hv4;
+        hv4.x = Hs[(jp + 0) * 66 + b_loc];
+        hv4.y = Hs[(jp + 1) * 66 + b_loc];
+        hv4.z = Hs[(jp + 2) * 66 + b_loc];
+        hv4.w = Hs[(jp + 3) * 66 + b_loc];
+        *(float4*)&h_out[(size_t)b * PH + jbase + jp] = hv4;
+        if (EXTRA_MODE == 1) {
+            u16* e = (u16*)extra;
+            *(uint2*)&e[(size_t)b * ex_stride + jbase + jp] =
+                make_uint2((u32)bf_rne(hv4.x) | ((u32)bf_rne(hv4.y) << 16),
+                           (u32)bf_rne(hv4.z) | ((u32)bf_rne(hv4.w) << 16));
+        } else if (EXTRA_MODE == 2) {
+            float* e = (float*)extra;
+            *(float4*)&e[(size_t)b * ex_stride + jbase + jp] = hv4;
+        }
+    }
 }
 
 template<class C>
@@ -836,7 +918,7 @@
 
 static const size_t BIG = (size_t)PS * PB * PH;
 
-static void run_mfma2(const Inputs& in, float* out, void* d_ws, hipStream_t stream)
+static void run_persistent(const Inputs& in, float* out, void* d_ws, hipStream_t stream)
 {
     char* p = (char*)d_ws;
     auto alloc = [&](size_t bytes) { char* r = p; p += bytes; return r; };
@@ -860,6 +942,7 @@
     float* q    = (float*)alloc((size_t)PB * PH * 4);
     float* catreg = (float*)alloc((size_t)PB * 2 * PH * 4 * 2);
     float* cur  = (float*)alloc((size_t)PB * PD * 4);
+    unsigned* bars = (unsigned*)alloc(256);
 
     u16* ctw_h     = (u16*)(W1e_reg + 0);
     u16* ctw_l     = (u16*)(W1e_reg + 1048576);
@@ -869,8 +952,8 @@
     u16* whh_d_lo  = (u16*)(W1e_reg + 8388608);
     float* hpp1    = (float*)(W1e_reg + 10485760);
     float* whh_f32p = catreg;
-    float* cat[2] = { catreg, catreg + (size_t)PB * 2 * PH };
-    float* hpp[2] = { hpp0, hpp1 };
+    float* cat0 = catreg;
+    float* cat1 = catreg + (size_t)PB * 2 * PH;
 
     prep_whh<<<P4H, 256, 0, stream>>>(in.enc_Whh, whh_e_hi, whh_e_lo, nullptr);
     prep_whh<<<P4H, 256, 0, stream>>>(in.dec_Whh, whh_d_hi, whh_d_lo, whh_f32p);
@@ -882,35 +965,23 @@
     gemm_wtA<1, 2><<<dim3(P4H / 64, (2 * PH) / 64), 256, 0, stream>>>(
         ctw_h, ctw_l, whh_f32p, nullptr, wf_h, wf_l, PH, 2 * PH);
     prep_bfused<<<P4H / 4, 256, 0, stream>>>(whh_f32p, in.comb_b, bsum_d, b_fus);
-    init_kernel<<<1024, 256, 0, stream>>>(hpp0, cT, cur);
-
-    for (int s = 0; s < PS; ++s) {
-        lstm_fused32<1, PH><<<dim3(P4H / 32, PB / 64), 256, 0, stream>>>(
-            whh_e_hi, whh_e_lo, wih_e, bsum_e,
-            in.inp + s * PD, PS * PD,
-            hpp[s & 1], cT, hpp[(s + 1) & 1],
-            enc_out + (size_t)s * PH, PS * PH);
-    }
+    init_kernel2<<<1024, 256, 0, stream>>>(hpp0, cT, cur, bars);
+
+    encoder_persistent<<<NBLK, 256, 0, stream>>>(
+        whh_e_hi, whh_e_lo, wih_e, bsum_e, in.inp,
+        hpp0, hpp1, cT, enc_out, bars);
 
     lstm_fused32<2, PH><<<dim3(P4H / 32, PB / 64), 256, 0, stream>>>(
         whh_d_hi, whh_d_lo, wih_d, bsum_d,
-        cur, PD, hpp[0], cT, h0, cat[1] + PH, 2 * PH);
+        cur, PD, hpp0, cT, h0, cat1 + PH, 2 * PH);
 
     gemm_wtA<0, 1><<<dim3((PS * PB) / 64, PH / 64), 256, 0, stream>>>(
         w1h, w1l, enc_out, in.b1, W1e, nullptr, PH, PH);
 
-    for (int t = 0; t < PS; ++t) {
-        float* cat_out = cat[(t + 1) & 1];
-        if (t > 0) {
-            lstm_fused32<2, 2 * PH><<<dim3(P4H / 32, PB / 64), 256, 0, stream>>>(
-                wf_h, wf_l, wih_d, b_fus,
-                cur, PD, cat[t & 1], cT, h0, cat_out + PH, 2 * PH);
-        }
-        gemm32_f32<<<dim3(PH / 32, PB / 32), 256, 0, stream>>>(
-            w2h, w2l, h0, in.b2, q, PH, PH);
-        attn_fused<<<PB, 256, 0, stream>>>(
-            W1e, enc_out, q, in.v_w, in.v_b, in.inp, out, cat_out, cur, t);
-    }
+    decoder_persistent<<<NBLK, 256, 0, stream>>>(
+        wf_h, wf_l, wih_d, b_fus, w2h, w2l, in.b2,
+        W1e, enc_out, in.v_w, in.v_b, in.inp,
+        cT, h0, q, cat0, cat1, cur, out, bars + 64);
 }
 
 static void run_mfma(const Inputs& in, float* out, void* d_ws, hipStream_t stream)
@@ -1035,7 +1106,8 @@
         (size_t)P4H * 4 * 3 +
         (size_t)PB * PH * 4 * 4 +
         (size_t)PB * 2 * PH * 4 * 2 +
-        (size_t)PB * PD * 4;
+        (size_t)PB * PD * 4 +
+        256;
     const size_t t2_need =
         BIG * 2 * 2 +
         (size_t)P4H * PH * 2 * 4 +
@@ -1049,7 +1121,7 @@
         ((size_t)PB * P4H + 4 * (size_t)PB * PH + (size_t)PB * 2 * PH +
          2 * (size_t)PB * PS + (size_t)PB * PD) * 4;
 
-    if (ws_size >= t1_need)       run_mfma2(in, out, d_ws, stream);
+    if (ws_size >= t1_need)       run_persistent(in, out, d_ws, stream);
     else if (ws_size >= t2_need)  run_mfma(in, out, d_ws, stream);
     else if (ws_size >= t3_need)  run_fallback(in, out, d_ws, stream);
 }
```

After: 38.98 ms. +261.2%, slower.
